# Optimization experiments

Hardware: AMD Instinct MI355X
Metric: run time of the kernel (lower is better)

## Reference

```python
import jax, jax.numpy as jnp
import numpy as np
import math

N_HEADS = 8
TANH_CLIP = 10.0
TEMP = 1.0


def setup_inputs() -> dict:
    key = jax.random.key(0)
    ks = jax.random.split(key, 8)
    B, N, D = 256, 2048, 128
    node_embeddings = jax.random.normal(ks[0], (B, N, D), dtype=jnp.float32)
    W_node = jax.random.normal(ks[1], (D, 3 * D), dtype=jnp.float32) / math.sqrt(D)
    W_fixed = jax.random.normal(ks[2], (D, D), dtype=jnp.float32) / math.sqrt(D)
    W_step = jax.random.normal(ks[3], (2 * D, D), dtype=jnp.float32) / math.sqrt(2 * D)
    W_out = jax.random.normal(ks[4], (D, D), dtype=jnp.float32) / math.sqrt(D)
    first_idx = jax.random.randint(ks[5], (B,), 0, N, dtype=jnp.int32)
    last_idx = jax.random.randint(ks[6], (B,), 0, N, dtype=jnp.int32)
    mask = jax.random.bernoulli(ks[7], 0.5, (B, N))
    mask = mask.at[:, 0].set(False)  # guarantee at least one feasible node per row
    return {"node_embeddings": node_embeddings, "W_node": W_node, "W_fixed": W_fixed,
            "W_step": W_step, "W_out": W_out, "first_idx": first_idx,
            "last_idx": last_idx, "mask": mask}


def reference(node_embeddings, W_node, W_fixed, W_step, W_out, first_idx, last_idx, mask):
    B, N, D = node_embeddings.shape
    H = N_HEADS
    hd = D // H  # key_dim = val_dim = embed_dim / n_heads
    neg_inf = -jnp.inf

    # --- _precompute ---
    graph_embed = node_embeddings.mean(axis=1)                # [B, D]
    fixed_context = graph_embed @ W_fixed                     # [B, D]
    proj = node_embeddings @ W_node                           # [B, N, 3D]
    gK, gV, logit_K = jnp.split(proj, 3, axis=-1)             # each [B, N, D]
    gK = gK.reshape(B, N, H, hd).transpose(2, 0, 1, 3)        # [H, B, N, hd]
    gV = gV.reshape(B, N, H, hd).transpose(2, 0, 1, 3)        # [H, B, N, hd]

    # --- step context: cat(first node emb, last node emb) ---
    first_emb = jnp.take_along_axis(node_embeddings, first_idx[:, None, None].astype(jnp.int32), axis=1)[:, 0]  # [B, D]
    last_emb = jnp.take_along_axis(node_embeddings, last_idx[:, None, None].astype(jnp.int32), axis=1)[:, 0]
    step_ctx = jnp.concatenate([first_emb, last_emb], axis=-1)  # [B, 2D]
    query = fixed_context + step_ctx @ W_step                 # [B, D]

    # --- glimpse multi-head attention (n_query = 1, masked inner) ---
    Q = query.reshape(B, H, hd).transpose(1, 0, 2)            # [H, B, hd]
    compat = jnp.einsum('hbd,hbnd->hbn', Q, gK) / math.sqrt(hd)  # [H, B, N]
    compat = jnp.where(mask[None, :, :], neg_inf, compat)     # mask_inner=True
    attn = jax.nn.softmax(compat, axis=-1)
    heads = jnp.einsum('hbn,hbnd->hbd', attn, gV)             # [H, B, hd]
    glimpse = heads.transpose(1, 0, 2).reshape(B, D) @ W_out  # project_out, [B, D]

    # --- logits with tanh clipping and masking ---
    logits = jnp.einsum('bd,bnd->bn', glimpse, logit_K) / math.sqrt(D)  # [B, N]
    logits = jnp.tanh(logits) * TANH_CLIP
    logits = jnp.where(mask, neg_inf, logits)                 # mask_logits=True
    log_p = jax.nn.log_softmax(logits / TEMP, axis=-1)        # [B, N]
    return log_p
```

## Files before the change

kernel.cpp:

```cpp
#include <hip/hip_runtime.h>
#include <math.h>

#define B_ 256
#define N_ 2048
#define D_ 128
#define GRID_F 1024

#define NEG_HUGE (-1.0e30f)

#define WSE_BYTES ((size_t)B_ * N_ * D_ * 2)
#define WSQ_OFF 262144
#define WSA_OFF 524288
#define WSB_OFF_M 2654208
#define WSC_OFF_M 2658304
#define FLAGS_OFF 2691072
#define WS_NEED_BYTES (WSE_BYTES + (size_t)(FLAGS_OFF + 1280) * 4)

#define WSA_STRIDE 1040
#define FB_WSB_OFF (B_ * 8 * WSA_STRIDE)
#define FB_WSC_OFF (FB_WSB_OFF + B_ * 8 * 2)

typedef __attribute__((ext_vector_type(8))) short bf16x8;
typedef __attribute__((ext_vector_type(4))) float f32x4;
typedef __attribute__((ext_vector_type(4))) unsigned short u16x4;
typedef __attribute__((ext_vector_type(2))) int i32x2;

__device__ __forceinline__ float wave_max64(float v) {
#pragma unroll
  for (int off = 32; off > 0; off >>= 1) v = fmaxf(v, __shfl_xor(v, off, 64));
  return v;
}
__device__ __forceinline__ float wave_sum64(float v) {
#pragma unroll
  for (int off = 32; off > 0; off >>= 1) v += __shfl_xor(v, off, 64);
  return v;
}
__device__ __forceinline__ unsigned short bf16rne(float f) {
  unsigned u = __float_as_uint(f);
  u += 0x7FFFu + ((u >> 16) & 1u);
  return (unsigned short)(u >> 16);
}
__device__ __forceinline__ float bflo(unsigned u) { return __uint_as_float(u << 16); }
__device__ __forceinline__ float bfhi(unsigned u) { return __uint_as_float(u & 0xFFFF0000u); }

__device__ __forceinline__ void do_A(const float* __restrict__ emb,
                                     unsigned short* __restrict__ wsE,
                                     float* __restrict__ wsM, int b, int s, int t,
                                     unsigned char* smem) {
  const int f4 = t & 31, gg = t >> 5;
  const size_t rowbase = (size_t)b * N_;
  float4 acc = make_float4(0.f, 0.f, 0.f, 0.f);
  int n = s * 256 + gg;
#pragma unroll 8
  for (int i = 0; i < 32; ++i, n += 8) {
    const float4 v = *(const float4*)(emb + (rowbase + n) * D_ + f4 * 4);
    acc.x += v.x; acc.y += v.y; acc.z += v.z; acc.w += v.w;
    ushort4 o;
    o.x = bf16rne(v.x); o.y = bf16rne(v.y); o.z = bf16rne(v.z); o.w = bf16rne(v.w);
    *(ushort4*)(wsE + (rowbase + n) * D_ + f4 * 4) = o;
  }
  float4* red = (float4*)smem;
  __syncthreads();
  red[t] = acc;
  __syncthreads();
  if (gg == 0) {
    float4 r = red[f4];
#pragma unroll
    for (int j = 1; j < 8; ++j) {
      const float4 a = red[j * 32 + f4];
      r.x += a.x; r.y += a.y; r.z += a.z; r.w += a.w;
    }
    *(float4*)(wsM + (size_t)(b * 8 + s) * 128 + f4 * 4) = r;
  }
}

__device__ __forceinline__ void do_B(const float* __restrict__ emb,
                                     const float* __restrict__ Wfix,
                                     const float* __restrict__ Wstep,
                                     const float* __restrict__ Wnode,
                                     const int* __restrict__ fidx,
                                     const int* __restrict__ lidx,
                                     const float* __restrict__ wsM,
                                     float* __restrict__ wsQ, int b, int t,
                                     unsigned char* smem) {
  float* ge = (float*)smem;
  float* fe = ge + 128;
  float* le = ge + 256;
  float* pq = ge + 384;
  float* q = ge + 640;
  if (t < 128) {
    float ssum = 0.f;
#pragma unroll
    for (int i = 0; i < 8; ++i) ssum += wsM[(size_t)(b * 8 + i) * 128 + t];
    ge[t] = ssum * (1.0f / 2048.0f);
    fe[t] = emb[((size_t)b * N_ + fidx[b]) * D_ + t];
    le[t] = emb[((size_t)b * N_ + lidx[b]) * D_ + t];
  }
  __syncthreads();
  {
    const int j = t & 127, h2 = t >> 7;
    float acc = 0.f;
#pragma unroll 4
    for (int k = 64 * h2; k < 64 * h2 + 64; ++k) {
      acc = fmaf(ge[k], Wfix[k * 128 + j], acc);
      acc = fmaf(fe[k], Wstep[k * 128 + j], acc);
      acc = fmaf(le[k], Wstep[(128 + k) * 128 + j], acc);
    }
    pq[h2 * 128 + j] = acc;
  }
  __syncthreads();
  if (t < 128) q[t] = pq[t] + pq[128 + t];
  __syncthreads();
  if (t < 128) {
    const float* wrow = Wnode + (size_t)t * 384;
#pragma unroll
    for (int h = 0; h < 8; ++h) {
      float a = 0.f;
#pragma unroll
      for (int k = 0; k < 16; ++k) a = fmaf(q[h * 16 + k], wrow[h * 16 + k], a);
      wsQ[(size_t)b * 1024 + h * 128 + t] = a * 0.25f;
    }
  }
}

__device__ __forceinline__ void do_C(const unsigned short* __restrict__ wsE,
                                     const unsigned char* __restrict__ mask,
                                     const float* __restrict__ wsQ,
                                     float* __restrict__ wsA, int b, int s, int t,
                                     unsigned char* smem) {
  unsigned short* eR = (unsigned short*)smem;
  unsigned short* pT = (unsigned short*)(smem + 18432);
  float* red0 = (float*)(smem + 20736);
  float* red1 = (float*)(smem + 20992);
  float* resc = (float*)(smem + 21248);
  unsigned char* mask_s = smem + 21312;
  const int lane = t & 63, w = t >> 6;
  const int lg = lane >> 4, lc = lane & 15;

  bf16x8 bq[4];
#pragma unroll
  for (int ks = 0; ks < 4; ++ks)
#pragma unroll
    for (int j = 0; j < 8; ++j) bq[ks][j] = 0;
  if (lc < 8) {
    const float* qrow = wsQ + (size_t)b * 1024 + lc * 128;
#pragma unroll
    for (int ks = 0; ks < 4; ++ks)
#pragma unroll
      for (int j = 0; j < 8; ++j)
        bq[ks][j] = (short)bf16rne(qrow[32 * ks + 8 * lg + j]);
  }

  float m_run = -INFINITY, l_run = 0.f;
  f32x4 wacc0 = {0.f, 0.f, 0.f, 0.f}, wacc1 = {0.f, 0.f, 0.f, 0.f};
  const unsigned short* embB = wsE + ((size_t)b * N_ + s * 256) * D_;
  const unsigned char* mrow = mask + (size_t)b * N_ + s * 256;

  for (int tile = 0; tile < 4; ++tile) {
    __syncthreads();
#pragma unroll
    for (int i = 0; i < 4; ++i) {
      const int gid = t + 256 * i;
      const int n = gid >> 4, d0 = (gid & 15) * 8;
      const int widx = ((n >> 2) * 8 + (d0 >> 4)) * 72 + ((n & 3) << 4) + (d0 & 15);
      const uint4 u = *(const uint4*)(embB + ((size_t)tile * 64 + n) * D_ + d0);
      *(uint4*)&eR[widx] = u;
    }
    if (t < 64) mask_s[t] = mrow[tile * 64 + t];
    __syncthreads();

    f32x4 sAcc = {0.f, 0.f, 0.f, 0.f};
#pragma unroll
    for (int ks = 0; ks < 4; ++ks) {
      const int aidx = ((4 * w + (lc >> 2)) * 8 + 2 * ks + (lg >> 1)) * 72 +
                       ((lc & 3) << 4) + ((lg & 1) << 3);
      const bf16x8 af = *(const bf16x8*)&eR[aidx];
      sAcc = __builtin_amdgcn_mfma_f32_16x16x32_bf16(af, bq[ks], sAcc, 0, 0, 0);
    }

    float sv[4];
    bool mk[4];
    float tmax = -INFINITY;
#pragma unroll
    for (int r = 0; r < 4; ++r) {
      mk[r] = mask_s[16 * w + 4 * lg + r] != 0;
      sv[r] = mk[r] ? -INFINITY : sAcc[r];
      tmax = fmaxf(tmax, sv[r]);
    }
    tmax = fmaxf(tmax, __shfl_xor(tmax, 16, 64));
    tmax = fmaxf(tmax, __shfl_xor(tmax, 32, 64));
    if (lane < 16) red0[w * 16 + lc] = tmax;
    __syncthreads();

    const float m_tile = fmaxf(fmaxf(red0[lc], red0[16 + lc]),
                               fmaxf(red0[32 + lc], red0[48 + lc]));
    const float m_new = fmaxf(m_run, m_tile);
    const float rsc = (m_new == -INFINITY) ? 1.f : __expf(m_run - m_new);
    float psum = 0.f;
    unsigned short pu[4];
#pragma unroll
    for (int r = 0; r < 4; ++r) {
      const float p = mk[r] ? 0.f : __expf(sv[r] - m_new);
      psum += p;
      pu[r] = bf16rne(p);
    }
    m_run = m_new;
    psum += __shfl_xor(psum, 16, 64);
    psum += __shfl_xor(psum, 32, 64);
    if (lane < 16) red1[w * 16 + lc] = psum;
    *(u16x4*)&pT[lc * 72 + 16 * w + 4 * lg] = (u16x4){pu[0], pu[1], pu[2], pu[3]};
    if (t < 16) resc[t] = rsc;
    __syncthreads();

    l_run = l_run * rsc + (red1[lc] + red1[16 + lc] + red1[32 + lc] + red1[48 + lc]);
    {
      const float r0f = resc[4 * lg + 0], r1f = resc[4 * lg + 1];
      const float r2f = resc[4 * lg + 2], r3f = resc[4 * lg + 3];
      wacc0[0] *= r0f; wacc0[1] *= r1f; wacc0[2] *= r2f; wacc0[3] *= r3f;
      wacc1[0] *= r0f; wacc1[1] *= r1f; wacc1[2] *= r2f; wacc1[3] *= r3f;
    }

    i32x2 tb0a, tb0b, tb1a, tb1b, tb2a, tb2b, tb3a, tb3b;
    {
      const unsigned base00 = (unsigned)(unsigned long long)
          &eR[((0 + 2 * lg) * 8 + w) * 72 + lc];
      const unsigned base01 = (unsigned)(unsigned long long)
          &eR[((0 + 2 * lg) * 8 + (w + 4)) * 72 + lc];
      const unsigned base10 = (unsigned)(unsigned long long)
          &eR[((8 + 2 * lg) * 8 + w) * 72 + lc];
      const unsigned base11 = (unsigned)(unsigned long long)
          &eR[((8 + 2 * lg) * 8 + (w + 4)) * 72 + lc];
      asm volatile("ds_read_b64_tr_b16 %0, %2 offset:0\n\t"
                   "ds_read_b64_tr_b16 %1, %2 offset:1152"
                   : "=v"(tb0a), "=v"(tb0b) : "v"(base00));
      asm volatile("ds_read_b64_tr_b16 %0, %2 offset:0\n\t"
                   "ds_read_b64_tr_b16 %1, %2 offset:1152"
                   : "=v"(tb1a), "=v"(tb1b) : "v"(base01));
      asm volatile("ds_read_b64_tr_b16 %0, %2 offset:0\n\t"
                   "ds_read_b64_tr_b16 %1, %2 offset:1152"
                   : "=v"(tb2a), "=v"(tb2b) : "v"(base10));
      asm volatile("ds_read_b64_tr_b16 %0, %2 offset:0\n\t"
                   "ds_read_b64_tr_b16 %1, %2 offset:1152"
                   : "=v"(tb3a), "=v"(tb3b) : "v"(base11));
      asm volatile("s_waitcnt lgkmcnt(0)" ::: "memory");
      __builtin_amdgcn_sched_barrier(0);
    }
    {
      const bf16x8 pa0 = *(const bf16x8*)&pT[lc * 72 + 8 * lg];
      const bf16x8 pa1 = *(const bf16x8*)&pT[lc * 72 + 32 + 8 * lg];
      union { i32x2 d[2]; bf16x8 v; } u;
      u.d[0] = tb0a; u.d[1] = tb0b;
      wacc0 = __builtin_amdgcn_mfma_f32_16x16x32_bf16(pa0, u.v, wacc0, 0, 0, 0);
      u.d[0] = tb1a; u.d[1] = tb1b;
      wacc1 = __builtin_amdgcn_mfma_f32_16x16x32_bf16(pa0, u.v, wacc1, 0, 0, 0);
      u.d[0] = tb2a; u.d[1] = tb2b;
      wacc0 = __builtin_amdgcn_mfma_f32_16x16x32_bf16(pa1, u.v, wacc0, 0, 0, 0);
      u.d[0] = tb3a; u.d[1] = tb3b;
      wacc1 = __builtin_amdgcn_mfma_f32_16x16x32_bf16(pa1, u.v, wacc1, 0, 0, 0);
    }
    __syncthreads();
  }

  float* dst = wsA + (size_t)(b * 8 + s) * WSA_STRIDE;
  if (lg < 2) {
#pragma unroll
    for (int r = 0; r < 4; ++r) {
      const int h = 4 * lg + r;
      dst[16 + h * 128 + 16 * w + lc] = wacc0[r];
      dst[16 + h * 128 + 16 * (w + 4) + lc] = wacc1[r];
    }
  }
  if (t < 8) { dst[t] = m_run; dst[8 + t] = l_run; }
}

__device__ __forceinline__ void do_D(const float* __restrict__ Wnode,
                                     const float* __restrict__ Wout,
                                     const float* __restrict__ wsA,
                                     float* __restrict__ wsC, int b, int t,
                                     unsigned char* smem) {
  float* Ls = (float*)smem;
  float* scale = Ls + 8;
  float* wl = scale + 64;
  float* heads = wl + 1024;
  float* glim = heads + 128;
  float* p2 = glim + 128;
  const int j = t & 127, hh = t >> 7;
  const float* base = wsA + (size_t)b * 8 * WSA_STRIDE;

  if (t < 8) {
    float M = -INFINITY;
#pragma unroll
    for (int s = 0; s < 8; ++s) M = fmaxf(M, base[s * WSA_STRIDE + t]);
    float L = 0.f;
#pragma unroll
    for (int s = 0; s < 8; ++s) {
      const float m = base[s * WSA_STRIDE + t];
      const float sc = (m == -INFINITY) ? 0.f : __expf(m - M);
      scale[s * 8 + t] = sc;
      L = fmaf(base[s * WSA_STRIDE + 8 + t], sc, L);
    }
    Ls[t] = L;
  }
  __syncthreads();
#pragma unroll
  for (int k = 0; k < 4; ++k) {
    const int idx = t + 256 * k;
    const int h = idx >> 7, d = idx & 127;
    float acc = 0.f;
#pragma unroll
    for (int s = 0; s < 8; ++s)
      acc = fmaf(scale[s * 8 + h], base[s * WSA_STRIDE + 16 + h * 128 + d], acc);
    wl[idx] = acc;
  }
  __syncthreads();
  {
    const int h = j >> 4, kk = j & 15;
    const float* wp = Wnode + 128 + h * 16 + kk;
    float acc = 0.f;
#pragma unroll 8
    for (int d = 64 * hh; d < 64 * hh + 64; ++d)
      acc = fmaf(wl[h * 128 + d], wp[(size_t)d * 384], acc);
    p2[hh * 128 + j] = acc;
  }
  __syncthreads();
  if (t < 128) heads[t] = (p2[t] + p2[128 + t]) / Ls[t >> 4];
  __syncthreads();
  {
    float acc = 0.f;
#pragma unroll 8
    for (int k = 64 * hh; k < 64 * hh + 64; ++k)
      acc = fmaf(heads[k], Wout[(size_t)k * 128 + j], acc);
    p2[hh * 128 + j] = acc;
  }
  __syncthreads();
  if (t < 128) glim[t] = p2[t] + p2[128 + t];
  __syncthreads();
  {
    const float* wr = Wnode + (size_t)j * 384 + 256;
    float acc = 0.f;
#pragma unroll 8
    for (int k = 64 * hh; k < 64 * hh + 64; ++k) acc = fmaf(wr[k], glim[k], acc);
    p2[hh * 128 + j] = acc;
  }
  __syncthreads();
  if (t < 128)
    wsC[(size_t)b * 128 + t] = (p2[t] + p2[128 + t]) * 0.08838834764831845f;
}

__device__ __forceinline__ void do_E(const unsigned short* __restrict__ wsE,
                                     const unsigned char* __restrict__ mask,
                                     const float* __restrict__ wsC,
                                     float* __restrict__ buf,
                                     float* __restrict__ wsB, int b, int s, int t,
                                     unsigned char* smem) {
  float* lgs = (float*)smem;
  const int lane = t & 63, w4 = t >> 6;
  const float4* c4 = (const float4*)(wsC + (size_t)b * 128);
  const float4 cfa = c4[(t & 15) * 2];
  const float4 cfb = c4[(t & 15) * 2 + 1];
  const unsigned short* embB = wsE + ((size_t)b * N_ + s * 256) * D_;
  const unsigned char* mrow = mask + (size_t)b * N_ + s * 256;
  float mr = NEG_HUGE, sr = 0.f;
  for (int tile = 0; tile < 4; ++tile) {
    const int n0 = tile * 64;
#pragma unroll
    for (int i = 0; i < 4; ++i) {
      const int gid = t + 256 * i;
      const int r = gid >> 4, c8 = (gid & 15) * 8;
      const uint4 u = *(const uint4*)(embB + (size_t)(n0 + r) * D_ + c8);
      float p = bflo(u.x) * cfa.x + bfhi(u.x) * cfa.y;
      p = fmaf(bflo(u.y), cfa.z, p); p = fmaf(bfhi(u.y), cfa.w, p);
      p = fmaf(bflo(u.z), cfb.x, p); p = fmaf(bfhi(u.z), cfb.y, p);
      p = fmaf(bflo(u.w), cfb.z, p); p = fmaf(bfhi(u.w), cfb.w, p);
      p += __shfl_xor(p, 8, 64);
      p += __shfl_xor(p, 4, 64);
      p += __shfl_xor(p, 2, 64);
      p += __shfl_xor(p, 1, 64);
      if ((t & 15) == 0) lgs[r] = p;
    }
    __syncthreads();
    const bool mk = mrow[n0 + lane] != 0;
    const float x = lgs[lane];
    const float ex = __expf(2.f * x);
    const float val = mk ? NEG_HUGE : (10.f - __fdividef(20.f, ex + 1.f));
    const float tm = wave_max64(val);
    const float mn = fmaxf(mr, tm);
    sr = sr * __expf(mr - mn) + wave_sum64(mk ? 0.f : __expf(val - mn));
    mr = mn;
    if (w4 == 0) buf[(size_t)b * N_ + s * 256 + n0 + lane] = val;
    __syncthreads();
  }
  if (t == 0) {
    wsB[(size_t)(b * 8 + s) * 2] = mr;
    wsB[(size_t)(b * 8 + s) * 2 + 1] = sr;
  }
}

__device__ __forceinline__ void do_F(const float* __restrict__ wsB,
                                     float* __restrict__ buf, int b, int t) {
  float M = NEG_HUGE;
#pragma unroll
  for (int q = 0; q < 8; ++q) M = fmaxf(M, wsB[(size_t)(b * 8 + q) * 2]);
  float S = 0.f;
#pragma unroll
  for (int q = 0; q < 8; ++q) {
    const float m = wsB[(size_t)(b * 8 + q) * 2];
    S += wsB[(size_t)(b * 8 + q) * 2 + 1] * __expf(m - M);
  }
  const float LS = M + logf(S);
#pragma unroll
  for (int i = 0; i < 8; ++i) {
    const size_t idx = (size_t)b * N_ + i * 256 + t;
    const float v = buf[idx];
    buf[idx] = (v <= -1.0e29f) ? NEG_HUGE : (v - LS);
  }
}

__global__ void __launch_bounds__(256, 4) k_flow(
    const float* __restrict__ emb, const float* __restrict__ Wnode,
    const float* __restrict__ Wfix, const float* __restrict__ Wstep,
    const float* __restrict__ Wout, const int* __restrict__ fidx,
    const int* __restrict__ lidx, const unsigned char* __restrict__ mask,
    float* __restrict__ buf, unsigned short* __restrict__ wsE,
    float* __restrict__ wsF, unsigned* __restrict__ flg) {
  const int g = blockIdx.x, t = threadIdx.x;
  float* wsM = wsF;
  float* wsQ = wsF + WSQ_OFF;
  float* wsA = wsF + WSA_OFF;
  float* wsB = wsF + WSB_OFF_M;
  float* wsC = wsF + WSC_OFF_M;
  unsigned* aprog = flg;
  unsigned* qrdy = flg + 256;
  unsigned* cprog = flg + 512;
  unsigned* crdy = flg + 768;
  unsigned* eprog = flg + 1024;

  __shared__ __align__(16) unsigned char smem[21504];
  __shared__ unsigned sh_old;

#pragma unroll 1
  for (int pass = 0; pass < 2; ++pass) {
    const int seg = g + GRID_F * pass;
    const int b = seg >> 3, s = seg & 7;

    do_A(emb, wsE, wsM, b, s, t, smem);
    __syncthreads();
    if (t == 0) { __threadfence(); sh_old = atomicAdd(&aprog[b], 1u); }
    __syncthreads();
    if (sh_old == 7u) {
      do_B(emb, Wfix, Wstep, Wnode, fidx, lidx, wsM, wsQ, b, t, smem);
      __syncthreads();
      if (t == 0) { __threadfence(); atomicExch(&qrdy[b], 1u); }
    }

    if (t == 0) {
      while (atomicAdd(&qrdy[b], 0u) == 0u) __builtin_amdgcn_s_sleep(8);
      __threadfence();
    }
    __syncthreads();
    do_C(wsE, mask, wsQ, wsA, b, s, t, smem);
    __syncthreads();
    if (t == 0) { __threadfence(); sh_old = atomicAdd(&cprog[b], 1u); }
    __syncthreads();
    if (sh_old == 7u) {
      do_D(Wnode, Wout, wsA, wsC, b, t, smem);
      __syncthreads();
      if (t == 0) { __threadfence(); atomicExch(&crdy[b], 1u); }
    }

    if (t == 0) {
      while (atomicAdd(&crdy[b], 0u) == 0u) __builtin_amdgcn_s_sleep(8);
      __threadfence();
    }
    __syncthreads();
    do_E(wsE, mask, wsC, buf, wsB, b, s, t, smem);
    __syncthreads();
    if (t == 0) { __threadfence(); sh_old = atomicAdd(&eprog[b], 1u); }
    __syncthreads();
    if (sh_old == 7u) do_F(wsB, buf, b, t);
    __syncthreads();
  }
}

__global__ void __launch_bounds__(256) k_prep(const float* __restrict__ emb,
                                              float* __restrict__ buf) {
  const int b = blockIdx.x, s = blockIdx.y, t = threadIdx.x;
  const int f4 = t & 31, g = t >> 5;
  const size_t rowbase = (size_t)b * N_;
  float4 acc = make_float4(0.f, 0.f, 0.f, 0.f);
  int n = s * 256 + g;
#pragma unroll 8
  for (int i = 0; i < 32; ++i, n += 8) {
    const float4 v = *(const float4*)(emb + (rowbase + n) * D_ + f4 * 4);
    acc.x += v.x; acc.y += v.y; acc.z += v.z; acc.w += v.w;
  }
  __shared__ float4 red[256];
  red[t] = acc;
  __syncthreads();
  if (g == 0) {
    float4 r = red[f4];
#pragma unroll
    for (int j = 1; j < 8; ++j) {
      const float4 a = red[j * 32 + f4];
      r.x += a.x; r.y += a.y; r.z += a.z; r.w += a.w;
    }
    *(float4*)(buf + (size_t)b * N_ + s * 128 + f4 * 4) = r;
  }
}

__global__ void __launch_bounds__(384) k_query(const float* __restrict__ emb,
                                               const float* __restrict__ Wfix,
                                               const float* __restrict__ Wstep,
                                               const float* __restrict__ Wnode,
                                               const int* __restrict__ fidx,
                                               const int* __restrict__ lidx,
                                               float* __restrict__ buf) {
  const int b = blockIdx.x, t = threadIdx.x;
  __shared__ float x[384];
  __shared__ float part[3][128];
  __shared__ float q[128];
  if (t < 128) {
    float ssum = 0.f;
#pragma unroll
    for (int i = 0; i < 8; ++i) ssum += buf[(size_t)b * N_ + i * 128 + t];
    x[t] = ssum * (1.0f / 2048.0f);
  } else if (t < 256) {
    x[t] = emb[((size_t)b * N_ + fidx[b]) * D_ + (t - 128)];
  } else {
    x[t] = emb[((size_t)b * N_ + lidx[b]) * D_ + (t - 256)];
  }
  __syncthreads();
  {
    const int seg = t >> 7, j = t & 127;
    const float* xs = &x[seg * 128];
    const float* Wp = (seg == 0) ? (Wfix + j) : (Wstep + (seg == 1 ? 0 : 128 * 128) + j);
    float acc = 0.f;
#pragma unroll 8
    for (int k = 0; k < 128; ++k) acc = fmaf(xs[k], Wp[(size_t)k * 128], acc);
    part[seg][j] = acc;
  }
  __syncthreads();
  if (t < 128) q[t] = part[0][t] + part[1][t] + part[2][t];
  __syncthreads();
  if (t < 128) {
    const float* wrow = Wnode + (size_t)t * 384;
#pragma unroll
    for (int h = 0; h < 8; ++h) {
      float a = 0.f;
#pragma unroll
      for (int k = 0; k < 16; ++k) a = fmaf(q[h * 16 + k], wrow[h * 16 + k], a);
      buf[(size_t)b * N_ + 1024 + h * 128 + t] = a * 0.25f;
    }
  }
}

__global__ void __launch_bounds__(256) k_attn_m(const float* __restrict__ emb,
                                                const unsigned char* __restrict__ mask,
                                                const float* __restrict__ buf,
                                                float* __restrict__ wsA) {
  const int b = blockIdx.x, s = blockIdx.y;
  const int t = threadIdx.x;
  const int lane = t & 63, w = t >> 6;
  const int lg = lane >> 4, lc = lane & 15;
  __shared__ __align__(16) unsigned char smem[21504];
  unsigned short* eR = (unsigned short*)smem;
  bf16x8 bq[4];
#pragma unroll
  for (int ks = 0; ks < 4; ++ks)
#pragma unroll
    for (int j = 0; j < 8; ++j) bq[ks][j] = 0;
  if (lc < 8) {
    const float* qrow = buf + (size_t)b * N_ + 1024 + lc * 128;
#pragma unroll
    for (int ks = 0; ks < 4; ++ks)
#pragma unroll
      for (int j = 0; j < 8; ++j)
        bq[ks][j] = (short)bf16rne(qrow[32 * ks + 8 * lg + j]);
  }
  unsigned short* pT = (unsigned short*)(smem + 18432);
  float* red0 = (float*)(smem + 20736);
  float* red1 = (float*)(smem + 20992);
  float* resc = (float*)(smem + 21248);
  unsigned char* mask_s = smem + 21312;
  float m_run = -INFINITY, l_run = 0.f;
  f32x4 wacc0 = {0.f, 0.f, 0.f, 0.f}, wacc1 = {0.f, 0.f, 0.f, 0.f};
  const float* embb = emb + ((size_t)b * N_ + s * 256) * D_;
  const unsigned char* mrow = mask + (size_t)b * N_ + s * 256;
  for (int tile = 0; tile < 4; ++tile) {
    {
      const float* src = embb + (size_t)tile * 64 * D_;
#pragma unroll
      for (int i = 0; i < 4; ++i) {
        const int gid = t + 256 * i;
        const int n = gid >> 4, d0 = (gid & 15) * 8;
        const float4 v0 = *(const float4*)(src + (size_t)n * D_ + d0);
        const float4 v1 = *(const float4*)(src + (size_t)n * D_ + d0 + 4);
        bf16x8 ev;
        ev[0] = (short)bf16rne(v0.x); ev[1] = (short)bf16rne(v0.y);
        ev[2] = (short)bf16rne(v0.z); ev[3] = (short)bf16rne(v0.w);
        ev[4] = (short)bf16rne(v1.x); ev[5] = (short)bf16rne(v1.y);
        ev[6] = (short)bf16rne(v1.z); ev[7] = (short)bf16rne(v1.w);
        const int widx = ((n >> 2) * 8 + (d0 >> 4)) * 72 + ((n & 3) << 4) + (d0 & 15);
        *(bf16x8*)&eR[widx] = ev;
      }
      if (t < 64) mask_s[t] = mrow[tile * 64 + t];
    }
    __syncthreads();
    f32x4 sAcc = {0.f, 0.f, 0.f, 0.f};
#pragma unroll
    for (int ks = 0; ks < 4; ++ks) {
      const int aidx = ((4 * w + (lc >> 2)) * 8 + 2 * ks + (lg >> 1)) * 72 +
                       ((lc & 3) << 4) + ((lg & 1) << 3);
      const bf16x8 af = *(const bf16x8*)&eR[aidx];
      sAcc = __builtin_amdgcn_mfma_f32_16x16x32_bf16(af, bq[ks], sAcc, 0, 0, 0);
    }
    float sv[4];
    bool mk[4];
    float tmax = -INFINITY;
#pragma unroll
    for (int r = 0; r < 4; ++r) {
      mk[r] = mask_s[16 * w + 4 * lg + r] != 0;
      sv[r] = mk[r] ? -INFINITY : sAcc[r];
      tmax = fmaxf(tmax, sv[r]);
    }
    tmax = fmaxf(tmax, __shfl_xor(tmax, 16, 64));
    tmax = fmaxf(tmax, __shfl_xor(tmax, 32, 64));
    if (lane < 16) red0[w * 16 + lc] = tmax;
    __syncthreads();
    const float m_tile = fmaxf(fmaxf(red0[lc], red0[16 + lc]),
                               fmaxf(red0[32 + lc], red0[48 + lc]));
    const float m_new = fmaxf(m_run, m_tile);
    const float rsc = (m_new == -INFINITY) ? 1.f : __expf(m_run - m_new);
    float psum = 0.f;
    unsigned short pu[4];
#pragma unroll
    for (int r = 0; r < 4; ++r) {
      const float p = mk[r] ? 0.f : __expf(sv[r] - m_new);
      psum += p;
      pu[r] = bf16rne(p);
    }
    m_run = m_new;
    psum += __shfl_xor(psum, 16, 64);
    psum += __shfl_xor(psum, 32, 64);
    if (lane < 16) red1[w * 16 + lc] = psum;
    *(u16x4*)&pT[lc * 72 + 16 * w + 4 * lg] = (u16x4){pu[0], pu[1], pu[2], pu[3]};
    if (t < 16) resc[t] = rsc;
    __syncthreads();
    l_run = l_run * rsc + (red1[lc] + red1[16 + lc] + red1[32 + lc] + red1[48 + lc]);
    {
      const float r0f = resc[4 * lg + 0], r1f = resc[4 * lg + 1];
      const float r2f = resc[4 * lg + 2], r3f = resc[4 * lg + 3];
      wacc0[0] *= r0f; wacc0[1] *= r1f; wacc0[2] *= r2f; wacc0[3] *= r3f;
      wacc1[0] *= r0f; wacc1[1] *= r1f; wacc1[2] *= r2f; wacc1[3] *= r3f;
    }
    i32x2 tb0a, tb0b, tb1a, tb1b, tb2a, tb2b, tb3a, tb3b;
    {
      const unsigned base00 = (unsigned)(unsigned long long)
          &eR[((0 + 2 * lg) * 8 + w) * 72 + lc];
      const unsigned base01 = (unsigned)(unsigned long long)
          &eR[((0 + 2 * lg) * 8 + (w + 4)) * 72 + lc];
      const unsigned base10 = (unsigned)(unsigned long long)
          &eR[((8 + 2 * lg) * 8 + w) * 72 + lc];
      const unsigned base11 = (unsigned)(unsigned long long)
          &eR[((8 + 2 * lg) * 8 + (w + 4)) * 72 + lc];
      asm volatile("ds_read_b64_tr_b16 %0, %2 offset:0\n\t"
                   "ds_read_b64_tr_b16 %1, %2 offset:1152"
                   : "=v"(tb0a), "=v"(tb0b) : "v"(base00));
      asm volatile("ds_read_b64_tr_b16 %0, %2 offset:0\n\t"
                   "ds_read_b64_tr_b16 %1, %2 offset:1152"
                   : "=v"(tb1a), "=v"(tb1b) : "v"(base01));
      asm volatile("ds_read_b64_tr_b16 %0, %2 offset:0\n\t"
                   "ds_read_b64_tr_b16 %1, %2 offset:1152"
                   : "=v"(tb2a), "=v"(tb2b) : "v"(base10));
      asm volatile("ds_read_b64_tr_b16 %0, %2 offset:0\n\t"
                   "ds_read_b64_tr_b16 %1, %2 offset:1152"
                   : "=v"(tb3a), "=v"(tb3b) : "v"(base11));
      asm volatile("s_waitcnt lgkmcnt(0)" ::: "memory");
      __builtin_amdgcn_sched_barrier(0);
    }
    {
      const bf16x8 pa0 = *(const bf16x8*)&pT[lc * 72 + 8 * lg];
      const bf16x8 pa1 = *(const bf16x8*)&pT[lc * 72 + 32 + 8 * lg];
      union { i32x2 d[2]; bf16x8 v; } u;
      u.d[0] = tb0a; u.d[1] = tb0b;
      wacc0 = __builtin_amdgcn_mfma_f32_16x16x32_bf16(pa0, u.v, wacc0, 0, 0, 0);
      u.d[0] = tb1a; u.d[1] = tb1b;
      wacc1 = __builtin_amdgcn_mfma_f32_16x16x32_bf16(pa0, u.v, wacc1, 0, 0, 0);
      u.d[0] = tb2a; u.d[1] = tb2b;
      wacc0 = __builtin_amdgcn_mfma_f32_16x16x32_bf16(pa1, u.v, wacc0, 0, 0, 0);
      u.d[0] = tb3a; u.d[1] = tb3b;
      wacc1 = __builtin_amdgcn_mfma_f32_16x16x32_bf16(pa1, u.v, wacc1, 0, 0, 0);
    }
    __syncthreads();
  }
  float* dst = wsA + (size_t)(b * 8 + s) * WSA_STRIDE;
  if (lg < 2) {
#pragma unroll
    for (int r = 0; r < 4; ++r) {
      const int h = 4 * lg + r;
      dst[16 + h * 128 + 16 * w + lc] = wacc0[r];
      dst[16 + h * 128 + 16 * (w + 4) + lc] = wacc1[r];
    }
  }
  if (t < 8) { dst[t] = m_run; dst[8 + t] = l_run; }
}

__global__ void __launch_bounds__(256) k_attn_comb(const float* __restrict__ Wnode,
                                                   const float* __restrict__ Wout,
                                                   const float* __restrict__ wsA,
                                                   float* __restrict__ wsC) {
  __shared__ __align__(16) unsigned char smem[10240];
  do_D(Wnode, Wout, wsA, wsC, blockIdx.x, threadIdx.x, smem);
}

__global__ void __launch_bounds__(256) k_logits_part(const float* __restrict__ emb,
                                                     const unsigned char* __restrict__ mask,
                                                     const float* __restrict__ wsC,
                                                     float* __restrict__ buf,
                                                     float* __restrict__ wsB) {
  const int b = blockIdx.x, s = blockIdx.y;
  const int t = threadIdx.x, lane = t & 63, w = t >> 6;
  __shared__ float lg[64];
  const float4 cf = ((const float4*)(wsC + (size_t)b * 128))[t & 31];
  const float* embb = emb + ((size_t)b * N_ + s * 256) * D_;
  const unsigned char* mrow = mask + (size_t)b * N_ + s * 256;
  float mr = NEG_HUGE, sr = 0.f;
  for (int tile = 0; tile < 4; ++tile) {
    const int n0 = tile * 64;
#pragma unroll
    for (int i = 0; i < 8; ++i) {
      const int gid = t + 256 * i;
      const int r = gid >> 5, c = (gid & 31) * 4;
      const float4 e = *(const float4*)(embb + (size_t)(n0 + r) * D_ + c);
      float p = fmaf(e.x, cf.x, fmaf(e.y, cf.y, fmaf(e.z, cf.z, e.w * cf.w)));
      p += __shfl_xor(p, 16, 64);
      p += __shfl_xor(p, 8, 64);
      p += __shfl_xor(p, 4, 64);
      p += __shfl_xor(p, 2, 64);
      p += __shfl_xor(p, 1, 64);
      if ((t & 31) == 0) lg[r] = p;
    }
    __syncthreads();
    const bool mk = mrow[n0 + lane] != 0;
    const float x = lg[lane];
    const float ex = __expf(2.f * x);
    const float val = mk ? NEG_HUGE : (10.f - __fdividef(20.f, ex + 1.f));
    const float tm = wave_max64(val);
    const float mn = fmaxf(mr, tm);
    sr = sr * __expf(mr - mn) + wave_sum64(mk ? 0.f : __expf(val - mn));
    mr = mn;
    if (w == 0) buf[(size_t)b * N_ + s * 256 + n0 + lane] = val;
    __syncthreads();
  }
  if (t == 0) {
    wsB[(size_t)(b * 8 + s) * 2] = mr;
    wsB[(size_t)(b * 8 + s) * 2 + 1] = sr;
  }
}

__global__ void __launch_bounds__(256) k_norm(const float* __restrict__ wsB,
                                              float* __restrict__ buf) {
  const int b = blockIdx.x, s = blockIdx.y, t = threadIdx.x;
  float M = NEG_HUGE;
#pragma unroll
  for (int q = 0; q < 8; ++q) M = fmaxf(M, wsB[(size_t)(b * 8 + q) * 2]);
  float S = 0.f;
#pragma unroll
  for (int q = 0; q < 8; ++q) {
    const float m = wsB[(size_t)(b * 8 + q) * 2];
    S += wsB[(size_t)(b * 8 + q) * 2 + 1] * __expf(m - M);
  }
  const float LS = M + logf(S);
  const size_t idx = (size_t)b * N_ + s * 256 + t;
  const float v = buf[idx];
  buf[idx] = (v <= -1.0e29f) ? NEG_HUGE : (v - LS);
}

extern "C" void kernel_launch(void* const* d_in, const int* in_sizes, int n_in,
                              void* d_out, int out_size, void* d_ws, size_t ws_size,
                              hipStream_t stream) {
  (void)in_sizes; (void)n_in; (void)out_size;
  const float* emb = (const float*)d_in[0];
  const float* Wnode = (const float*)d_in[1];
  const float* Wfix = (const float*)d_in[2];
  const float* Wstep = (const float*)d_in[3];
  const float* Wout = (const float*)d_in[4];
  const int* fidx = (const int*)d_in[5];
  const int* lidx = (const int*)d_in[6];
  const unsigned char* mask = (const unsigned char*)d_in[7];
  float* buf = (float*)d_out;

  int occ = 0;
  (void)hipOccupancyMaxActiveBlocksPerMultiprocessor(&occ, k_flow, 256, 0);

  if (occ >= 4 && ws_size >= WS_NEED_BYTES) {
    unsigned short* wsE = (unsigned short*)d_ws;
    float* wsF = (float*)((char*)d_ws + WSE_BYTES);
    unsigned* flg = (unsigned*)(wsF + FLAGS_OFF);
    hipMemsetAsync(flg, 0, 1280 * 4, stream);
    k_flow<<<GRID_F, 256, 0, stream>>>(emb, Wnode, Wfix, Wstep, Wout, fidx,
                                       lidx, mask, buf, wsE, wsF, flg);
  } else {
    float* ws = (float*)d_ws;
    k_prep<<<dim3(B_, 8), 256, 0, stream>>>(emb, buf);
    k_query<<<B_, 384, 0, stream>>>(emb, Wfix, Wstep, Wnode, fidx, lidx, buf);
    k_attn_m<<<dim3(B_, 8), 256, 0, stream>>>(emb, mask, buf, ws);
    k_attn_comb<<<B_, 256, 0, stream>>>(Wnode, Wout, ws, ws + FB_WSC_OFF);
    k_logits_part<<<dim3(B_, 8), 256, 0, stream>>>(emb, mask, ws + FB_WSC_OFF, buf,
                                                   ws + FB_WSB_OFF);
    k_norm<<<dim3(B_, 8), 256, 0, stream>>>(ws + FB_WSB_OFF, buf);
  }
}
```

Baseline: 160.3 us.

## Keep bf16 segment in LDS across fused persistent passes instead of global workspace

Replaces the persistent flow kernel, which staged a bf16 copy of all embeddings in global workspace, with a fused kernel. Each block converts a 256-node segment into a 72KB LDS buffer and reuses it for the mean, the attention and the logits phases within the same pass. This removes the global bf16 write and its two re-reads, leaving one read of the fp32 input. The cost is lower occupancy (2 blocks per CU, grid of 512), so each block runs 4 passes. Each pass also spin-waits on per-batch flags, which risks stalls while that segment's LDS buffer stays resident.

```diff
diff --git a/kernel.cpp b/kernel.cpp
--- a/kernel.cpp
+++ b/kernel.cpp
@@ -4,17 +4,16 @@
 #define B_ 256
 #define N_ 2048
 #define D_ 128
-#define GRID_F 1024
+#define GRID_F 512
 
 #define NEG_HUGE (-1.0e30f)
 
-#define WSE_BYTES ((size_t)B_ * N_ * D_ * 2)
 #define WSQ_OFF 262144
 #define WSA_OFF 524288
 #define WSB_OFF_M 2654208
 #define WSC_OFF_M 2658304
 #define FLAGS_OFF 2691072
-#define WS_NEED_BYTES (WSE_BYTES + (size_t)(FLAGS_OFF + 1280) * 4)
+#define WS_NEED_BYTES ((size_t)(FLAGS_OFF + 1280) * 4)
 
 #define WSA_STRIDE 1040
 #define FB_WSB_OFF (B_ * 8 * WSA_STRIDE)
@@ -43,73 +42,479 @@
 __device__ __forceinline__ float bflo(unsigned u) { return __uint_as_float(u << 16); }
 __device__ __forceinline__ float bfhi(unsigned u) { return __uint_as_float(u & 0xFFFF0000u); }
 
-__device__ __forceinline__ void do_A(const float* __restrict__ emb,
-                                     unsigned short* __restrict__ wsE,
-                                     float* __restrict__ wsM, int b, int s, int t,
+__device__ __forceinline__ void do_D(const float* __restrict__ Wnode,
+                                     const float* __restrict__ Wout,
+                                     const float* __restrict__ wsA,
+                                     float* __restrict__ wsC, int b, int t,
                                      unsigned char* smem) {
-  const int f4 = t & 31, gg = t >> 5;
+  float* Ls = (float*)smem;
+  float* scale = Ls + 8;
+  float* wl = scale + 64;
+  float* heads = wl + 1024;
+  float* glim = heads + 128;
+  float* p2 = glim + 128;
+  const int j = t & 127, hh = t >> 7;
+  const float* base = wsA + (size_t)b * 8 * WSA_STRIDE;
+
+  if (t < 8) {
+    float M = -INFINITY;
+#pragma unroll
+    for (int s = 0; s < 8; ++s) M = fmaxf(M, base[s * WSA_STRIDE + t]);
+    float L = 0.f;
+#pragma unroll
+    for (int s = 0; s < 8; ++s) {
+      const float m = base[s * WSA_STRIDE + t];
+      const float sc = (m == -INFINITY) ? 0.f : __expf(m - M);
+      scale[s * 8 + t] = sc;
+      L = fmaf(base[s * WSA_STRIDE + 8 + t], sc, L);
+    }
+    Ls[t] = L;
+  }
+  __syncthreads();
+#pragma unroll
+  for (int k = 0; k < 4; ++k) {
+    const int idx = t + 256 * k;
+    const int h = idx >> 7, d = idx & 127;
+    float acc = 0.f;
+#pragma unroll
+    for (int s = 0; s < 8; ++s)
+      acc = fmaf(scale[s * 8 + h], base[s * WSA_STRIDE + 16 + h * 128 + d], acc);
+    wl[idx] = acc;
+  }
+  __syncthreads();
+  {
+    const int h = j >> 4, kk = j & 15;
+    const float* wp = Wnode + 128 + h * 16 + kk;
+    float acc = 0.f;
+#pragma unroll 8
+    for (int d = 64 * hh; d < 64 * hh + 64; ++d)
+      acc = fmaf(wl[h * 128 + d], wp[(size_t)d * 384], acc);
+    p2[hh * 128 + j] = acc;
+  }
+  __syncthreads();
+  if (t < 128) heads[t] = (p2[t] + p2[128 + t]) / Ls[t >> 4];
+  __syncthreads();
+  {
+    float acc = 0.f;
+#pragma unroll 8
+    for (int k = 64 * hh; k < 64 * hh + 64; ++k)
+      acc = fmaf(heads[k], Wout[(size_t)k * 128 + j], acc);
+    p2[hh * 128 + j] = acc;
+  }
+  __syncthreads();
+  if (t < 128) glim[t] = p2[t] + p2[128 + t];
+  __syncthreads();
+  {
+    const float* wr = Wnode + (size_t)j * 384 + 256;
+    float acc = 0.f;
+#pragma unroll 8
+    for (int k = 64 * hh; k < 64 * hh + 64; ++k) acc = fmaf(wr[k], glim[k], acc);
+    p2[hh * 128 + j] = acc;
+  }
+  __syncthreads();
+  if (t < 128)
+    wsC[(size_t)b * 128 + t] = (p2[t] + p2[128 + t]) * 0.08838834764831845f;
+  __syncthreads();
+}
+
+__global__ void __launch_bounds__(256, 2) k_fused(
+    const float* __restrict__ emb, const float* __restrict__ Wnode,
+    const float* __restrict__ Wfix, const float* __restrict__ Wstep,
+    const float* __restrict__ Wout, const int* __restrict__ fidx,
+    const int* __restrict__ lidx, const unsigned char* __restrict__ mask,
+    float* __restrict__ buf, float* __restrict__ wsF,
+    unsigned* __restrict__ flg) {
+  const int g = blockIdx.x, t = threadIdx.x;
+  float* wsM = wsF;
+  float* wsQ = wsF + WSQ_OFF;
+  float* wsA = wsF + WSA_OFF;
+  float* wsB = wsF + WSB_OFF_M;
+  float* wsC = wsF + WSC_OFF_M;
+  unsigned* aprog = flg;
+  unsigned* qrdy = flg + 256;
+  unsigned* cprog = flg + 512;
+  unsigned* crdy = flg + 768;
+  unsigned* eprog = flg + 1024;
+
+  __shared__ __align__(16) unsigned short eSeg[36864];
+  __shared__ __align__(16) unsigned char scratch[6464];
+  __shared__ unsigned sh_old;
+
+  const int lane = t & 63, w = t >> 6;
+  const int lg = lane >> 4, lc = lane & 15;
+
+#pragma unroll 1
+  for (int pass = 0; pass < 4; ++pass) {
+    const int seg = g + GRID_F * pass;
+    const int b = seg >> 3, s = seg & 7;
+    const float* src = emb + ((size_t)b * N_ + s * 256) * D_;
+    const unsigned char* mrow = mask + (size_t)b * N_ + s * 256;
+
+    {
+      const int d0 = (t & 15) * 8;
+      float p[8];
+#pragma unroll
+      for (int j = 0; j < 8; ++j) p[j] = 0.f;
+#pragma unroll
+      for (int i = 0; i < 16; ++i) {
+        const int n = (t >> 4) + 16 * i;
+        const float4 v0 = *(const float4*)(src + (size_t)n * D_ + d0);
+        const float4 v1 = *(const float4*)(src + (size_t)n * D_ + d0 + 4);
+        p[0] += v0.x; p[1] += v0.y; p[2] += v0.z; p[3] += v0.w;
+        p[4] += v1.x; p[5] += v1.y; p[6] += v1.z; p[7] += v1.w;
+        bf16x8 ev;
+        ev[0] = (short)bf16rne(v0.x); ev[1] = (short)bf16rne(v0.y);
+        ev[2] = (short)bf16rne(v0.z); ev[3] = (short)bf16rne(v0.w);
+        ev[4] = (short)bf16rne(v1.x); ev[5] = (short)bf16rne(v1.y);
+        ev[6] = (short)bf16rne(v1.z); ev[7] = (short)bf16rne(v1.w);
+        const int widx = ((n >> 2) * 8 + (d0 >> 4)) * 72 + ((n & 3) << 4) + (d0 & 15);
+        *(bf16x8*)&eSeg[widx] = ev;
+      }
+#pragma unroll
+      for (int j = 0; j < 8; ++j) {
+        p[j] += __shfl_xor(p[j], 16, 64);
+        p[j] += __shfl_xor(p[j], 32, 64);
+      }
+      float* red = (float*)scratch;
+      if (lane < 16) {
+        float* dstp = red + w * 128 + lane * 8;
+#pragma unroll
+        for (int j = 0; j < 8; ++j) dstp[j] = p[j];
+      }
+      __syncthreads();
+      if (t < 128)
+        wsM[(size_t)(b * 8 + s) * 128 + t] =
+            red[t] + red[128 + t] + red[256 + t] + red[384 + t];
+      __syncthreads();
+    }
+    if (t == 0) { __threadfence(); sh_old = atomicAdd(&aprog[b], 1u); }
+    __syncthreads();
+
+    if (sh_old == 7u) {
+      __threadfence();
+      float* ge = (float*)scratch;
+      float* fe = ge + 128;
+      float* le = ge + 256;
+      float* pq = ge + 384;
+      float* q = ge + 640;
+      if (t < 128) {
+        float ssum = 0.f;
+#pragma unroll
+        for (int i = 0; i < 8; ++i) ssum += wsM[(size_t)(b * 8 + i) * 128 + t];
+        ge[t] = ssum * (1.0f / 2048.0f);
+        fe[t] = emb[((size_t)b * N_ + fidx[b]) * D_ + t];
+        le[t] = emb[((size_t)b * N_ + lidx[b]) * D_ + t];
+      }
+      __syncthreads();
+      {
+        const int j = t & 127, h2 = t >> 7;
+        float acc = 0.f;
+#pragma unroll 4
+        for (int k = 64 * h2; k < 64 * h2 + 64; ++k) {
+          acc = fmaf(ge[k], Wfix[k * 128 + j], acc);
+          acc = fmaf(fe[k], Wstep[k * 128 + j], acc);
+          acc = fmaf(le[k], Wstep[(128 + k) * 128 + j], acc);
+        }
+        pq[h2 * 128 + j] = acc;
+      }
+      __syncthreads();
+      if (t < 128) q[t] = pq[t] + pq[128 + t];
+      __syncthreads();
+      if (t < 128) {
+        const float* wrow = Wnode + (size_t)t * 384;
+#pragma unroll
+        for (int h = 0; h < 8; ++h) {
+          float a = 0.f;
+#pragma unroll
+          for (int k = 0; k < 16; ++k) a = fmaf(q[h * 16 + k], wrow[h * 16 + k], a);
+          wsQ[(size_t)b * 1024 + h * 128 + t] = a * 0.25f;
+        }
+      }
+      __syncthreads();
+      if (t == 0) { __threadfence(); atomicExch(&qrdy[b], 1u); }
+    }
+
+    if (t == 0) {
+      while (atomicAdd(&qrdy[b], 0u) == 0u) __builtin_amdgcn_s_sleep(8);
+      __threadfence();
+    }
+    __syncthreads();
+    {
+      unsigned short* pT = (unsigned short*)scratch;
+      float* red0 = (float*)(scratch + 2304);
+      float* red1 = (float*)(scratch + 2560);
+      float* resc = (float*)(scratch + 2816);
+
+      bf16x8 bq[4];
+#pragma unroll
+      for (int ks = 0; ks < 4; ++ks)
+#pragma unroll
+        for (int j = 0; j < 8; ++j) bq[ks][j] = 0;
+      if (lc < 8) {
+        const float* qrow = wsQ + (size_t)b * 1024 + lc * 128;
+#pragma unroll
+        for (int ks = 0; ks < 4; ++ks)
+#pragma unroll
+          for (int j = 0; j < 8; ++j)
+            bq[ks][j] = (short)bf16rne(qrow[32 * ks + 8 * lg + j]);
+      }
+
+      float m_run = -INFINITY, l_run = 0.f;
+      f32x4 wacc0 = {0.f, 0.f, 0.f, 0.f}, wacc1 = {0.f, 0.f, 0.f, 0.f};
+
+      for (int tile = 0; tile < 4; ++tile) {
+        const unsigned short* eR = eSeg + tile * 9216;
+        __syncthreads();
+
+        f32x4 sAcc = {0.f, 0.f, 0.f, 0.f};
+#pragma unroll
+        for (int ks = 0; ks < 4; ++ks) {
+          const int aidx = ((4 * w + (lc >> 2)) * 8 + 2 * ks + (lg >> 1)) * 72 +
+                           ((lc & 3) << 4) + ((lg & 1) << 3);
+          const bf16x8 af = *(const bf16x8*)&eR[aidx];
+          sAcc = __builtin_amdgcn_mfma_f32_16x16x32_bf16(af, bq[ks], sAcc, 0, 0, 0);
+        }
+
+        float sv[4];
+        bool mk[4];
+        float tmax = -INFINITY;
+#pragma unroll
+        for (int r = 0; r < 4; ++r) {
+          mk[r] = mrow[tile * 64 + 16 * w + 4 * lg + r] != 0;
+          sv[r] = mk[r] ? -INFINITY : sAcc[r];
+          tmax = fmaxf(tmax, sv[r]);
+        }
+        tmax = fmaxf(tmax, __shfl_xor(tmax, 16, 64));
+        tmax = fmaxf(tmax, __shfl_xor(tmax, 32, 64));
+        if (lane < 16) red0[w * 16 + lc] = tmax;
+        __syncthreads();
+
+        const float m_tile = fmaxf(fmaxf(red0[lc], red0[16 + lc]),
+                                   fmaxf(red0[32 + lc], red0[48 + lc]));
+        const float m_new = fmaxf(m_run, m_tile);
+        const float rsc = (m_new == -INFINITY) ? 1.f : __expf(m_run - m_new);
+        float psum = 0.f;
+        unsigned short pu[4];
+#pragma unroll
+        for (int r = 0; r < 4; ++r) {
+          const float p = mk[r] ? 0.f : __expf(sv[r] - m_new);
+          psum += p;
+          pu[r] = bf16rne(p);
+        }
+        m_run = m_new;
+        psum += __shfl_xor(psum, 16, 64);
+        psum += __shfl_xor(psum, 32, 64);
+        if (lane < 16) red1[w * 16 + lc] = psum;
+        *(u16x4*)&pT[lc * 72 + 16 * w + 4 * lg] = (u16x4){pu[0], pu[1], pu[2], pu[3]};
+        if (t < 16) resc[t] = rsc;
+        __syncthreads();
+
+        l_run = l_run * rsc +
+                (red1[lc] + red1[16 + lc] + red1[32 + lc] + red1[48 + lc]);
+        {
+          const float r0f = resc[4 * lg + 0], r1f = resc[4 * lg + 1];
+          const float r2f = resc[4 * lg + 2], r3f = resc[4 * lg + 3];
+          wacc0[0] *= r0f; wacc0[1] *= r1f; wacc0[2] *= r2f; wacc0[3] *= r3f;
+          wacc1[0] *= r0f; wacc1[1] *= r1f; wacc1[2] *= r2f; wacc1[3] *= r3f;
+        }
+
+        i32x2 tb0a, tb0b, tb1a, tb1b, tb2a, tb2b, tb3a, tb3b;
+        {
+          const unsigned base00 = (unsigned)(unsigned long long)
+              &eR[((0 + 2 * lg) * 8 + w) * 72 + lc];
+          const unsigned base01 = (unsigned)(unsigned long long)
+              &eR[((0 + 2 * lg) * 8 + (w + 4)) * 72 + lc];
+          const unsigned base10 = (unsigned)(unsigned long long)
+              &eR[((8 + 2 * lg) * 8 + w) * 72 + lc];
+          const unsigned base11 = (unsigned)(unsigned long long)
+              &eR[((8 + 2 * lg) * 8 + (w + 4)) * 72 + lc];
+          asm volatile("ds_read_b64_tr_b16 %0, %2 offset:0\n\t"
+                       "ds_read_b64_tr_b16 %1, %2 offset:1152"
+                       : "=v"(tb0a), "=v"(tb0b) : "v"(base00));
+          asm volatile("ds_read_b64_tr_b16 %0, %2 offset:0\n\t"
+                       "ds_read_b64_tr_b16 %1, %2 offset:1152"
+                       : "=v"(tb1a), "=v"(tb1b) : "v"(base01));
+          asm volatile("ds_read_b64_tr_b16 %0, %2 offset:0\n\t"
+                       "ds_read_b64_tr_b16 %1, %2 offset:1152"
+                       : "=v"(tb2a), "=v"(tb2b) : "v"(base10));
+          asm volatile("ds_read_b64_tr_b16 %0, %2 offset:0\n\t"
+                       "ds_read_b64_tr_b16 %1, %2 offset:1152"
+                       : "=v"(tb3a), "=v"(tb3b) : "v"(base11));
+          asm volatile("s_waitcnt lgkmcnt(0)" ::: "memory");
+          __builtin_amdgcn_sched_barrier(0);
+        }
+        {
+          const bf16x8 pa0 = *(const bf16x8*)&pT[lc * 72 + 8 * lg];
+          const bf16x8 pa1 = *(const bf16x8*)&pT[lc * 72 + 32 + 8 * lg];
+          union { i32x2 d[2]; bf16x8 v; } u;
+          u.d[0] = tb0a; u.d[1] = tb0b;
+          wacc0 = __builtin_amdgcn_mfma_f32_16x16x32_bf16(pa0, u.v, wacc0, 0, 0, 0);
+          u.d[0] = tb1a; u.d[1] = tb1b;
+          wacc1 = __builtin_amdgcn_mfma_f32_16x16x32_bf16(pa0, u.v, wacc1, 0, 0, 0);
+          u.d[0] = tb2a; u.d[1] = tb2b;
+          wacc0 = __builtin_amdgcn_mfma_f32_16x16x32_bf16(pa1, u.v, wacc0, 0, 0, 0);
+          u.d[0] = tb3a; u.d[1] = tb3b;
+          wacc1 = __builtin_amdgcn_mfma_f32_16x16x32_bf16(pa1, u.v, wacc1, 0, 0, 0);
+        }
+      }
+      __syncthreads();
+
+      float* dst = wsA + (size_t)(b * 8 + s) * WSA_STRIDE;
+      if (lg < 2) {
+#pragma unroll
+        for (int r = 0; r < 4; ++r) {
+          const int h = 4 * lg + r;
+          dst[16 + h * 128 + 16 * w + lc] = wacc0[r];
+          dst[16 + h * 128 + 16 * (w + 4) + lc] = wacc1[r];
+        }
+      }
+      if (t < 8) { dst[t] = m_run; dst[8 + t] = l_run; }
+    }
+    __syncthreads();
+    if (t == 0) { __threadfence(); sh_old = atomicAdd(&cprog[b], 1u); }
+    __syncthreads();
+
+    if (sh_old == 7u) {
+      __threadfence();
+      do_D(Wnode, Wout, wsA, wsC, b, t, scratch);
+      if (t == 0) { __threadfence(); atomicExch(&crdy[b], 1u); }
+    }
+
+    if (t == 0) {
+      while (atomicAdd(&crdy[b], 0u) == 0u) __builtin_amdgcn_s_sleep(8);
+      __threadfence();
+    }
+    __syncthreads();
+    {
+      float* lgs = (float*)scratch;
+      const float4* c4 = (const float4*)(wsC + (size_t)b * 128);
+      const float4 cfa = c4[(t & 15) * 2];
+      const float4 cfb = c4[(t & 15) * 2 + 1];
+      float mr = NEG_HUGE, sr = 0.f;
+      for (int tile = 0; tile < 4; ++tile) {
+        const int n0 = tile * 64;
+#pragma unroll
+        for (int i = 0; i < 4; ++i) {
+          const int gid = t + 256 * i;
+          const int r = gid >> 4, c8 = (gid & 15) * 8;
+          const int nn = n0 + r;
+          const int idx =
+              ((nn >> 2) * 8 + (c8 >> 4)) * 72 + ((nn & 3) << 4) + (c8 & 15);
+          const bf16x8 ev = *(const bf16x8*)&eSeg[idx];
+          const uint4 u = *(const uint4*)&ev;
+          float p = bflo(u.x) * cfa.x + bfhi(u.x) * cfa.y;
+          p = fmaf(bflo(u.y), cfa.z, p); p = fmaf(bfhi(u.y), cfa.w, p);
+          p = fmaf(bflo(u.z), cfb.x, p); p = fmaf(bfhi(u.z), cfb.y, p);
+          p = fmaf(bflo(u.w), cfb.z, p); p = fmaf(bfhi(u.w), cfb.w, p);
+          p += __shfl_xor(p, 8, 64);
+          p += __shfl_xor(p, 4, 64);
+          p += __shfl_xor(p, 2, 64);
+          p += __shfl_xor(p, 1, 64);
+          if ((t & 15) == 0) lgs[r] = p;
+        }
+        __syncthreads();
+        const bool mk = mrow[n0 + lane] != 0;
+        const float x = lgs[lane];
+        const float ex = __expf(2.f * x);
+        const float val = mk ? NEG_HUGE : (10.f - __fdividef(20.f, ex + 1.f));
+        const float tm = wave_max64(val);
+        const float mn = fmaxf(mr, tm);
+        sr = sr * __expf(mr - mn) + wave_sum64(mk ? 0.f : __expf(val - mn));
+        mr = mn;
+        if (w == 0) buf[(size_t)b * N_ + s * 256 + n0 + lane] = val;
+        __syncthreads();
+      }
+      if (t == 0) {
+        wsB[(size_t)(b * 8 + s) * 2] = mr;
+        wsB[(size_t)(b * 8 + s) * 2 + 1] = sr;
+      }
+    }
+    __syncthreads();
+    if (t == 0) { __threadfence(); sh_old = atomicAdd(&eprog[b], 1u); }
+    __syncthreads();
+
+    if (sh_old == 7u) {
+      __threadfence();
+      float M = NEG_HUGE;
+#pragma unroll
+      for (int q = 0; q < 8; ++q) M = fmaxf(M, wsB[(size_t)(b * 8 + q) * 2]);
+      float S = 0.f;
+#pragma unroll
+      for (int q = 0; q < 8; ++q) {
+        const float m = wsB[(size_t)(b * 8 + q) * 2];
+        S += wsB[(size_t)(b * 8 + q) * 2 + 1] * __expf(m - M);
+      }
+      const float LS = M + logf(S);
+#pragma unroll
+      for (int i = 0; i < 8; ++i) {
+        const size_t idx = (size_t)b * N_ + i * 256 + t;
+        const float v = buf[idx];
+        buf[idx] = (v <= -1.0e29f) ? NEG_HUGE : (v - LS);
+      }
+    }
+    __syncthreads();
+  }
+}
+
+__global__ void __launch_bounds__(256) k_prep(const float* __restrict__ emb,
+                                              float* __restrict__ buf) {
+  const int b = blockIdx.x, s = blockIdx.y, t = threadIdx.x;
+  const int f4 = t & 31, g = t >> 5;
   const size_t rowbase = (size_t)b * N_;
   float4 acc = make_float4(0.f, 0.f, 0.f, 0.f);
-  int n = s * 256 + gg;
+  int n = s * 256 + g;
 #pragma unroll 8
   for (int i = 0; i < 32; ++i, n += 8) {
     const float4 v = *(const float4*)(emb + (rowbase + n) * D_ + f4 * 4);
     acc.x += v.x; acc.y += v.y; acc.z += v.z; acc.w += v.w;
-    ushort4 o;
-    o.x = bf16rne(v.x); o.y = bf16rne(v.y); o.z = bf16rne(v.z); o.w = bf16rne(v.w);
-    *(ushort4*)(wsE + (rowbase + n) * D_ + f4 * 4) = o;
-  }
-  float4* red = (float4*)smem;
-  __syncthreads();
+  }
+  __shared__ float4 red[256];
   red[t] = acc;
   __syncthreads();
-  if (gg == 0) {
+  if (g == 0) {
     float4 r = red[f4];
 #pragma unroll
     for (int j = 1; j < 8; ++j) {
       const float4 a = red[j * 32 + f4];
       r.x += a.x; r.y += a.y; r.z += a.z; r.w += a.w;
     }
-    *(float4*)(wsM + (size_t)(b * 8 + s) * 128 + f4 * 4) = r;
-  }
-}
-
-__device__ __forceinline__ void do_B(const float* __restrict__ emb,
-                                     const float* __restrict__ Wfix,
-                                     const float* __restrict__ Wstep,
-                                     const float* __restrict__ Wnode,
-                                     const int* __restrict__ fidx,
-                                     const int* __restrict__ lidx,
-                                     const float* __restrict__ wsM,
-                                     float* __restrict__ wsQ, int b, int t,
-                                     unsigned char* smem) {
-  float* ge = (float*)smem;
-  float* fe = ge + 128;
-  float* le = ge + 256;
-  float* pq = ge + 384;
-  float* q = ge + 640;
+    *(float4*)(buf + (size_t)b * N_ + s * 128 + f4 * 4) = r;
+  }
+}
+
+__global__ void __launch_bounds__(384) k_query(const float* __restrict__ emb,
+                                               const float* __restrict__ Wfix,
+                                               const float* __restrict__ Wstep,
+                                               const float* __restrict__ Wnode,
+                                               const int* __restrict__ fidx,
+                                               const int* __restrict__ lidx,
+                                               float* __restrict__ buf) {
+  const int b = blockIdx.x, t = threadIdx.x;
+  __shared__ float x[384];
+  __shared__ float part[3][128];
+  __shared__ float q[128];
   if (t < 128) {
     float ssum = 0.f;
 #pragma unroll
-    for (int i = 0; i < 8; ++i) ssum += wsM[(size_t)(b * 8 + i) * 128 + t];
-    ge[t] = ssum * (1.0f / 2048.0f);
-    fe[t] = emb[((size_t)b * N_ + fidx[b]) * D_ + t];
-    le[t] = emb[((size_t)b * N_ + lidx[b]) * D_ + t];
+    for (int i = 0; i < 8; ++i) ssum += buf[(size_t)b * N_ + i * 128 + t];
+    x[t] = ssum * (1.0f / 2048.0f);
+  } else if (t < 256) {
+    x[t] = emb[((size_t)b * N_ + fidx[b]) * D_ + (t - 128)];
+  } else {
+    x[t] = emb[((size_t)b * N_ + lidx[b]) * D_ + (t - 256)];
   }
   __syncthreads();
   {
-    const int j = t & 127, h2 = t >> 7;
+    const int seg = t >> 7, j = t & 127;
+    const float* xs = &x[seg * 128];
+    const float* Wp = (seg == 0) ? (Wfix + j) : (Wstep + (seg == 1 ? 0 : 128 * 128) + j);
     float acc = 0.f;
-#pragma unroll 4
-    for (int k = 64 * h2; k < 64 * h2 + 64; ++k) {
-      acc = fmaf(ge[k], Wfix[k * 128 + j], acc);
-      acc = fmaf(fe[k], Wstep[k * 128 + j], acc);
-      acc = fmaf(le[k], Wstep[(128 + k) * 128 + j], acc);
-    }
-    pq[h2 * 128 + j] = acc;
-  }
-  __syncthreads();
-  if (t < 128) q[t] = pq[t] + pq[128 + t];
+#pragma unroll 8
+    for (int k = 0; k < 128; ++k) acc = fmaf(xs[k], Wp[(size_t)k * 128], acc);
+    part[seg][j] = acc;
+  }
+  __syncthreads();
+  if (t < 128) q[t] = part[0][t] + part[1][t] + part[2][t];
   __syncthreads();
   if (t < 128) {
     const float* wrow = Wnode + (size_t)t * 384;
@@ -118,57 +523,62 @@
       float a = 0.f;
 #pragma unroll
       for (int k = 0; k < 16; ++k) a = fmaf(q[h * 16 + k], wrow[h * 16 + k], a);
-      wsQ[(size_t)b * 1024 + h * 128 + t] = a * 0.25f;
-    }
-  }
-}
-
-__device__ __forceinline__ void do_C(const unsigned short* __restrict__ wsE,
-                                     const unsigned char* __restrict__ mask,
-                                     const float* __restrict__ wsQ,
-                                     float* __restrict__ wsA, int b, int s, int t,
-                                     unsigned char* smem) {
-  unsigned short* eR = (unsigned short*)smem;
-  unsigned short* pT = (unsigned short*)(smem + 18432);
-  float* red0 = (float*)(smem + 20736);
-  float* red1 = (float*)(smem + 20992);
-  float* resc = (float*)(smem + 21248);
-  unsigned char* mask_s = smem + 21312;
+      buf[(size_t)b * N_ + 1024 + h * 128 + t] = a * 0.25f;
+    }
+  }
+}
+
+__global__ void __launch_bounds__(256) k_attn_m(const float* __restrict__ emb,
+                                                const unsigned char* __restrict__ mask,
+                                                const float* __restrict__ buf,
+                                                float* __restrict__ wsA) {
+  const int b = blockIdx.x, s = blockIdx.y;
+  const int t = threadIdx.x;
   const int lane = t & 63, w = t >> 6;
   const int lg = lane >> 4, lc = lane & 15;
-
+  __shared__ __align__(16) unsigned short eR[9216];
+  __shared__ __align__(16) unsigned short pT[16 * 72];
+  __shared__ float red0[64];
+  __shared__ float red1[64];
+  __shared__ float resc[16];
+  __shared__ unsigned char mask_s[64];
   bf16x8 bq[4];
 #pragma unroll
   for (int ks = 0; ks < 4; ++ks)
 #pragma unroll
     for (int j = 0; j < 8; ++j) bq[ks][j] = 0;
   if (lc < 8) {
-    const float* qrow = wsQ + (size_t)b * 1024 + lc * 128;
+    const float* qrow = buf + (size_t)b * N_ + 1024 + lc * 128;
 #pragma unroll
     for (int ks = 0; ks < 4; ++ks)
 #pragma unroll
       for (int j = 0; j < 8; ++j)
         bq[ks][j] = (short)bf16rne(qrow[32 * ks + 8 * lg + j]);
   }
-
   float m_run = -INFINITY, l_run = 0.f;
   f32x4 wacc0 = {0.f, 0.f, 0.f, 0.f}, wacc1 = {0.f, 0.f, 0.f, 0.f};
-  const unsigned short* embB = wsE + ((size_t)b * N_ + s * 256) * D_;
+  const float* embb = emb + ((size_t)b * N_ + s * 256) * D_;
   const unsigned char* mrow = mask + (size_t)b * N_ + s * 256;
-
   for (int tile = 0; tile < 4; ++tile) {
-    __syncthreads();
-#pragma unroll
-    for (int i = 0; i < 4; ++i) {
-      const int gid = t + 256 * i;
-      const int n = gid >> 4, d0 = (gid & 15) * 8;
-      const int widx = ((n >> 2) * 8 + (d0 >> 4)) * 72 + ((n & 3) << 4) + (d0 & 15);
-      const uint4 u = *(const uint4*)(embB + ((size_t)tile * 64 + n) * D_ + d0);
-      *(uint4*)&eR[widx] = u;
-    }
-    if (t < 64) mask_s[t] = mrow[tile * 64 + t];
-    __syncthreads();
-
+    {
+      const float* src = embb + (size_t)tile * 64 * D_;
+#pragma unroll
+      for (int i = 0; i < 4; ++i) {
+        const int gid = t + 256 * i;
+        const int n = gid >> 4, d0 = (gid & 15) * 8;
+        const float4 v0 = *(const float4*)(src + (size_t)n * D_ + d0);
+        const float4 v1 = *(const float4*)(src + (size_t)n * D_ + d0 + 4);
+        bf16x8 ev;
+        ev[0] = (short)bf16rne(v0.x); ev[1] = (short)bf16rne(v0.y);
+        ev[2] = (short)bf16rne(v0.z); ev[3] = (short)bf16rne(v0.w);
+        ev[4] = (short)bf16rne(v1.x); ev[5] = (short)bf16rne(v1.y);
+        ev[6] = (short)bf16rne(v1.z); ev[7] = (short)bf16rne(v1.w);
+        const int widx = ((n >> 2) * 8 + (d0 >> 4)) * 72 + ((n & 3) << 4) + (d0 & 15);
+        *(bf16x8*)&eR[widx] = ev;
+      }
+      if (t < 64) mask_s[t] = mrow[tile * 64 + t];
+    }
+    __syncthreads();
     f32x4 sAcc = {0.f, 0.f, 0.f, 0.f};
 #pragma unroll
     for (int ks = 0; ks < 4; ++ks) {
@@ -177,7 +587,6 @@
       const bf16x8 af = *(const bf16x8*)&eR[aidx];
       sAcc = __builtin_amdgcn_mfma_f32_16x16x32_bf16(af, bq[ks], sAcc, 0, 0, 0);
     }
-
     float sv[4];
     bool mk[4];
     float tmax = -INFINITY;
@@ -191,7 +600,6 @@
     tmax = fmaxf(tmax, __shfl_xor(tmax, 32, 64));
     if (lane < 16) red0[w * 16 + lc] = tmax;
     __syncthreads();
-
     const float m_tile = fmaxf(fmaxf(red0[lc], red0[16 + lc]),
                                fmaxf(red0[32 + lc], red0[48 + lc]));
     const float m_new = fmaxf(m_run, m_tile);
@@ -211,7 +619,6 @@
     *(u16x4*)&pT[lc * 72 + 16 * w + 4 * lg] = (u16x4){pu[0], pu[1], pu[2], pu[3]};
     if (t < 16) resc[t] = rsc;
     __syncthreads();
-
     l_run = l_run * rsc + (red1[lc] + red1[16 + lc] + red1[32 + lc] + red1[48 + lc]);
     {
       const float r0f = resc[4 * lg + 0], r1f = resc[4 * lg + 1];
@@ -219,7 +626,6 @@
       wacc0[0] *= r0f; wacc0[1] *= r1f; wacc0[2] *= r2f; wacc0[3] *= r3f;
       wacc1[0] *= r0f; wacc1[1] *= r1f; wacc1[2] *= r2f; wacc1[3] *= r3f;
     }
-
     i32x2 tb0a, tb0b, tb1a, tb1b, tb2a, tb2b, tb3a, tb3b;
     {
       const unsigned base00 = (unsigned)(unsigned long long)
@@ -260,7 +666,6 @@
     }
     __syncthreads();
   }
-
   float* dst = wsA + (size_t)(b * 8 + s) * WSA_STRIDE;
   if (lg < 2) {
 #pragma unroll
@@ -273,443 +678,11 @@
   if (t < 8) { dst[t] = m_run; dst[8 + t] = l_run; }
 }
 
-__device__ __forceinline__ void do_D(const float* __restrict__ Wnode,
-                                     const float* __restrict__ Wout,
-                                     const float* __restrict__ wsA,
-                                     float* __restrict__ wsC, int b, int t,
-                                     unsigned char* smem) {
-  float* Ls = (float*)smem;
-  float* scale = Ls + 8;
-  float* wl = scale + 64;
-  float* heads = wl + 1024;
-  float* glim = heads + 128;
-  float* p2 = glim + 128;
-  const int j = t & 127, hh = t >> 7;
-  const float* base = wsA + (size_t)b * 8 * WSA_STRIDE;
-
-  if (t < 8) {
-    float M = -INFINITY;
-#pragma unroll
-    for (int s = 0; s < 8; ++s) M = fmaxf(M, base[s * WSA_STRIDE + t]);
-    float L = 0.f;
-#pragma unroll
-    for (int s = 0; s < 8; ++s) {
-      const float m = base[s * WSA_STRIDE + t];
-      const float sc = (m == -INFINITY) ? 0.f : __expf(m - M);
-      scale[s * 8 + t] = sc;
-      L = fmaf(base[s * WSA_STRIDE + 8 + t], sc, L);
-    }
-    Ls[t] = L;
-  }
-  __syncthreads();
-#pragma unroll
-  for (int k = 0; k < 4; ++k) {
-    const int idx = t + 256 * k;
-    const int h = idx >> 7, d = idx & 127;
-    float acc = 0.f;
-#pragma unroll
-    for (int s = 0; s < 8; ++s)
-      acc = fmaf(scale[s * 8 + h], base[s * WSA_STRIDE + 16 + h * 128 + d], acc);
-    wl[idx] = acc;
-  }
-  __syncthreads();
-  {
-    const int h = j >> 4, kk = j & 15;
-    const float* wp = Wnode + 128 + h * 16 + kk;
-    float acc = 0.f;
-#pragma unroll 8
-    for (int d = 64 * hh; d < 64 * hh + 64; ++d)
-      acc = fmaf(wl[h * 128 + d], wp[(size_t)d * 384], acc);
-    p2[hh * 128 + j] = acc;
-  }
-  __syncthreads();
-  if (t < 128) heads[t] = (p2[t] + p2[128 + t]) / Ls[t >> 4];
-  __syncthreads();
-  {
-    float acc = 0.f;
-#pragma unroll 8
-    for (int k = 64 * hh; k < 64 * hh + 64; ++k)
-      acc = fmaf(heads[k], Wout[(size_t)k * 128 + j], acc);
-    p2[hh * 128 + j] = acc;
-  }
-  __syncthreads();
-  if (t < 128) glim[t] = p2[t] + p2[128 + t];
-  __syncthreads();
-  {
-    const float* wr = Wnode + (size_t)j * 384 + 256;
-    float acc = 0.f;
-#pragma unroll 8
-    for (int k = 64 * hh; k < 64 * hh + 64; ++k) acc = fmaf(wr[k], glim[k], acc);
-    p2[hh * 128 + j] = acc;
-  }
-  __syncthreads();
-  if (t < 128)
-    wsC[(size_t)b * 128 + t] = (p2[t] + p2[128 + t]) * 0.08838834764831845f;
-}
-
-__device__ __forceinline__ void do_E(const unsigned short* __restrict__ wsE,
-                                     const unsigned char* __restrict__ mask,
-                                     const float* __restrict__ wsC,
-                                     float* __restrict__ buf,
-                                     float* __restrict__ wsB, int b, int s, int t,
-                                     unsigned char* smem) {
-  float* lgs = (float*)smem;
-  const int lane = t & 63, w4 = t >> 6;
-  const float4* c4 = (const float4*)(wsC + (size_t)b * 128);
-  const float4 cfa = c4[(t & 15) * 2];
-  const float4 cfb = c4[(t & 15) * 2 + 1];
-  const unsigned short* embB = wsE + ((size_t)b * N_ + s * 256) * D_;
-  const unsigned char* mrow = mask + (size_t)b * N_ + s * 256;
-  float mr = NEG_HUGE, sr = 0.f;
-  for (int tile = 0; tile < 4; ++tile) {
-    const int n0 = tile * 64;
-#pragma unroll
-    for (int i = 0; i < 4; ++i) {
-      const int gid = t + 256 * i;
-      const int r = gid >> 4, c8 = (gid & 15) * 8;
-      const uint4 u = *(const uint4*)(embB + (size_t)(n0 + r) * D_ + c8);
-      float p = bflo(u.x) * cfa.x + bfhi(u.x) * cfa.y;
-      p = fmaf(bflo(u.y), cfa.z, p); p = fmaf(bfhi(u.y), cfa.w, p);
-      p = fmaf(bflo(u.z), cfb.x, p); p = fmaf(bfhi(u.z), cfb.y, p);
-      p = fmaf(bflo(u.w), cfb.z, p); p = fmaf(bfhi(u.w), cfb.w, p);
-      p += __shfl_xor(p, 8, 64);
-      p += __shfl_xor(p, 4, 64);
-      p += __shfl_xor(p, 2, 64);
-      p += __shfl_xor(p, 1, 64);
-      if ((t & 15) == 0) lgs[r] = p;
-    }
-    __syncthreads();
-    const bool mk = mrow[n0 + lane] != 0;
-    const float x = lgs[lane];
-    const float ex = __expf(2.f * x);
-    const float val = mk ? NEG_HUGE : (10.f - __fdividef(20.f, ex + 1.f));
-    const float tm = wave_max64(val);
-    const float mn = fmaxf(mr, tm);
-    sr = sr * __expf(mr - mn) + wave_sum64(mk ? 0.f : __expf(val - mn));
-    mr = mn;
-    if (w4 == 0) buf[(size_t)b * N_ + s * 256 + n0 + lane] = val;
-    __syncthreads();
-  }
-  if (t == 0) {
-    wsB[(size_t)(b * 8 + s) * 2] = mr;
-    wsB[(size_t)(b * 8 + s) * 2 + 1] = sr;
-  }
-}
-
-__device__ __forceinline__ void do_F(const float* __restrict__ wsB,
-                                     float* __restrict__ buf, int b, int t) {
-  float M = NEG_HUGE;
-#pragma unroll
-  for (int q = 0; q < 8; ++q) M = fmaxf(M, wsB[(size_t)(b * 8 + q) * 2]);
-  float S = 0.f;
-#pragma unroll
-  for (int q = 0; q < 8; ++q) {
-    const float m = wsB[(size_t)(b * 8 + q) * 2];
-    S += wsB[(size_t)(b * 8 + q) * 2 + 1] * __expf(m - M);
-  }
-  const float LS = M + logf(S);
-#pragma unroll
-  for (int i = 0; i < 8; ++i) {
-    const size_t idx = (size_t)b * N_ + i * 256 + t;
-    const float v = buf[idx];
-    buf[idx] = (v <= -1.0e29f) ? NEG_HUGE : (v - LS);
-  }
-}
-
-__global__ void __launch_bounds__(256, 4) k_flow(
-    const float* __restrict__ emb, const float* __restrict__ Wnode,
-    const float* __restrict__ Wfix, const float* __restrict__ Wstep,
-    const float* __restrict__ Wout, const int* __restrict__ fidx,
-    const int* __restrict__ lidx, const unsigned char* __restrict__ mask,
-    float* __restrict__ buf, unsigned short* __restrict__ wsE,
-    float* __restrict__ wsF, unsigned* __restrict__ flg) {
-  const int g = blockIdx.x, t = threadIdx.x;
-  float* wsM = wsF;
-  float* wsQ = wsF + WSQ_OFF;
-  float* wsA = wsF + WSA_OFF;
-  float* wsB = wsF + WSB_OFF_M;
-  float* wsC = wsF + WSC_OFF_M;
-  unsigned* aprog = flg;
-  unsigned* qrdy = flg + 256;
-  unsigned* cprog = flg + 512;
-  unsigned* crdy = flg + 768;
-  unsigned* eprog = flg + 1024;
-
-  __shared__ __align__(16) unsigned char smem[21504];
-  __shared__ unsigned sh_old;
-
-#pragma unroll 1
-  for (int pass = 0; pass < 2; ++pass) {
-    const int seg = g + GRID_F * pass;
-    const int b = seg >> 3, s = seg & 7;
-
-    do_A(emb, wsE, wsM, b, s, t, smem);
-    __syncthreads();
-    if (t == 0) { __threadfence(); sh_old = atomicAdd(&aprog[b], 1u); }
-    __syncthreads();
-    if (sh_old == 7u) {
-      do_B(emb, Wfix, Wstep, Wnode, fidx, lidx, wsM, wsQ, b, t, smem);
-      __syncthreads();
-      if (t == 0) { __threadfence(); atomicExch(&qrdy[b], 1u); }
-    }
-
-    if (t == 0) {
-      while (atomicAdd(&qrdy[b], 0u) == 0u) __builtin_amdgcn_s_sleep(8);
-      __threadfence();
-    }
-    __syncthreads();
-    do_C(wsE, mask, wsQ, wsA, b, s, t, smem);
-    __syncthreads();
-    if (t == 0) { __threadfence(); sh_old = atomicAdd(&cprog[b], 1u); }
-    __syncthreads();
-    if (sh_old == 7u) {
-      do_D(Wnode, Wout, wsA, wsC, b, t, smem);
-      __syncthreads();
-      if (t == 0) { __threadfence(); atomicExch(&crdy[b], 1u); }
-    }
-
-    if (t == 0) {
-      while (atomicAdd(&crdy[b], 0u) == 0u) __builtin_amdgcn_s_sleep(8);
-      __threadfence();
-    }
-    __syncthreads();
-    do_E(wsE, mask, wsC, buf, wsB, b, s, t, smem);
-    __syncthreads();
-    if (t == 0) { __threadfence(); sh_old = atomicAdd(&eprog[b], 1u); }
-    __syncthreads();
-    if (sh_old == 7u) do_F(wsB, buf, b, t);
-    __syncthreads();
-  }
-}
-
-__global__ void __launch_bounds__(256) k_prep(const float* __restrict__ emb,
-                                              float* __restrict__ buf) {
-  const int b = blockIdx.x, s = blockIdx.y, t = threadIdx.x;
-  const int f4 = t & 31, g = t >> 5;
-  const size_t rowbase = (size_t)b * N_;
-  float4 acc = make_float4(0.f, 0.f, 0.f, 0.f);
-  int n = s * 256 + g;
-#pragma unroll 8
-  for (int i = 0; i < 32; ++i, n += 8) {
-    const float4 v = *(const float4*)(emb + (rowbase + n) * D_ + f4 * 4);
-    acc.x += v.x; acc.y += v.y; acc.z += v.z; acc.w += v.w;
-  }
-  __shared__ float4 red[256];
-  red[t] = acc;
-  __syncthreads();
-  if (g == 0) {
-    float4 r = red[f4];
-#pragma unroll
-    for (int j = 1; j < 8; ++j) {
-      const float4 a = red[j * 32 + f4];
-      r.x += a.x; r.y += a.y; r.z += a.z; r.w += a.w;
-    }
-    *(float4*)(buf + (size_t)b * N_ + s * 128 + f4 * 4) = r;
-  }
-}
-
-__global__ void __launch_bounds__(384) k_query(const float* __restrict__ emb,
-                                               const float* __restrict__ Wfix,
-                                               const float* __restrict__ Wstep,
-                                               const float* __restrict__ Wnode,
-                                               const int* __restrict__ fidx,
-                                               const int* __restrict__ lidx,
-                                               float* __restrict__ buf) {
-  const int b = blockIdx.x, t = threadIdx.x;
-  __shared__ float x[384];
-  __shared__ float part[3][128];
-  __shared__ float q[128];
-  if (t < 128) {
-    float ssum = 0.f;
-#pragma unroll
-    for (int i = 0; i < 8; ++i) ssum += buf[(size_t)b * N_ + i * 128 + t];
-    x[t] = ssum * (1.0f / 2048.0f);
-  } else if (t < 256) {
-    x[t] = emb[((size_t)b * N_ + fidx[b]) * D_ + (t - 128)];
-  } else {
-    x[t] = emb[((size_t)b * N_ + lidx[b]) * D_ + (t - 256)];
-  }
-  __syncthreads();
-  {
-    const int seg = t >> 7, j = t & 127;
-    const float* xs = &x[seg * 128];
-    const float* Wp = (seg == 0) ? (Wfix + j) : (Wstep + (seg == 1 ? 0 : 128 * 128) + j);
-    float acc = 0.f;
-#pragma unroll 8
-    for (int k = 0; k < 128; ++k) acc = fmaf(xs[k], Wp[(size_t)k * 128], acc);
-    part[seg][j] = acc;
-  }
-  __syncthreads();
-  if (t < 128) q[t] = part[0][t] + part[1][t] + part[2][t];
-  __syncthreads();
-  if (t < 128) {
-    const float* wrow = Wnode + (size_t)t * 384;
-#pragma unroll
-    for (int h = 0; h < 8; ++h) {
-      float a = 0.f;
-#pragma unroll
-      for (int k = 0; k < 16; ++k) a = fmaf(q[h * 16 + k], wrow[h * 16 + k], a);
-      buf[(size_t)b * N_ + 1024 + h * 128 + t] = a * 0.25f;
-    }
-  }
-}
-
-__global__ void __launch_bounds__(256) k_attn_m(const float* __restrict__ emb,
-                                                const unsigned char* __restrict__ mask,
-                                                const float* __restrict__ buf,
-                                                float* __restrict__ wsA) {
-  const int b = blockIdx.x, s = blockIdx.y;
-  const int t = threadIdx.x;
-  const int lane = t & 63, w = t >> 6;
-  const int lg = lane >> 4, lc = lane & 15;
-  __shared__ __align__(16) unsigned char smem[21504];
-  unsigned short* eR = (unsigned short*)smem;
-  bf16x8 bq[4];
-#pragma unroll
-  for (int ks = 0; ks < 4; ++ks)
-#pragma unroll
-    for (int j = 0; j < 8; ++j) bq[ks][j] = 0;
-  if (lc < 8) {
-    const float* qrow = buf + (size_t)b * N_ + 1024 + lc * 128;
-#pragma unroll
-    for (int ks = 0; ks < 4; ++ks)
-#pragma unroll
-      for (int j = 0; j < 8; ++j)
-        bq[ks][j] = (short)bf16rne(qrow[32 * ks + 8 * lg + j]);
-  }
-  unsigned short* pT = (unsigned short*)(smem + 18432);
-  float* red0 = (float*)(smem + 20736);
-  float* red1 = (float*)(smem + 20992);
-  float* resc = (float*)(smem + 21248);
-  unsigned char* mask_s = smem + 21312;
-  float m_run = -INFINITY, l_run = 0.f;
-  f32x4 wacc0 = {0.f, 0.f, 0.f, 0.f}, wacc1 = {0.f, 0.f, 0.f, 0.f};
-  const float* embb = emb + ((size_t)b * N_ + s * 256) * D_;
-  const unsigned char* mrow = mask + (size_t)b * N_ + s * 256;
-  for (int tile = 0; tile < 4; ++tile) {
-    {
-      const float* src = embb + (size_t)tile * 64 * D_;
-#pragma unroll
-      for (int i = 0; i < 4; ++i) {
-        const int gid = t + 256 * i;
-        const int n = gid >> 4, d0 = (gid & 15) * 8;
-        const float4 v0 = *(const float4*)(src + (size_t)n * D_ + d0);
-        const float4 v1 = *(const float4*)(src + (size_t)n * D_ + d0 + 4);
-        bf16x8 ev;
-        ev[0] = (short)bf16rne(v0.x); ev[1] = (short)bf16rne(v0.y);
-        ev[2] = (short)bf16rne(v0.z); ev[3] = (short)bf16rne(v0.w);
-        ev[4] = (short)bf16rne(v1.x); ev[5] = (short)bf16rne(v1.y);
-        ev[6] = (short)bf16rne(v1.z); ev[7] = (short)bf16rne(v1.w);
-        const int widx = ((n >> 2) * 8 + (d0 >> 4)) * 72 + ((n & 3) << 4) + (d0 & 15);
-        *(bf16x8*)&eR[widx] = ev;
-      }
-      if (t < 64) mask_s[t] = mrow[tile * 64 + t];
-    }
-    __syncthreads();
-    f32x4 sAcc = {0.f, 0.f, 0.f, 0.f};
-#pragma unroll
-    for (int ks = 0; ks < 4; ++ks) {
-      const int aidx = ((4 * w + (lc >> 2)) * 8 + 2 * ks + (lg >> 1)) * 72 +
-                       ((lc & 3) << 4) + ((lg & 1) << 3);
-      const bf16x8 af = *(const bf16x8*)&eR[aidx];
-      sAcc = __builtin_amdgcn_mfma_f32_16x16x32_bf16(af, bq[ks], sAcc, 0, 0, 0);
-    }
-    float sv[4];
-    bool mk[4];
-    float tmax = -INFINITY;
-#pragma unroll
-    for (int r = 0; r < 4; ++r) {
-      mk[r] = mask_s[16 * w + 4 * lg + r] != 0;
-      sv[r] = mk[r] ? -INFINITY : sAcc[r];
-      tmax = fmaxf(tmax, sv[r]);
-    }
-    tmax = fmaxf(tmax, __shfl_xor(tmax, 16, 64));
-    tmax = fmaxf(tmax, __shfl_xor(tmax, 32, 64));
-    if (lane < 16) red0[w * 16 + lc] = tmax;
-    __syncthreads();
-    const float m_tile = fmaxf(fmaxf(red0[lc], red0[16 + lc]),
-                               fmaxf(red0[32 + lc], red0[48 + lc]));
-    const float m_new = fmaxf(m_run, m_tile);
-    const float rsc = (m_new == -INFINITY) ? 1.f : __expf(m_run - m_new);
-    float psum = 0.f;
-    unsigned short pu[4];
-#pragma unroll
-    for (int r = 0; r < 4; ++r) {
-      const float p = mk[r] ? 0.f : __expf(sv[r] - m_new);
-      psum += p;
-      pu[r] = bf16rne(p);
-    }
-    m_run = m_new;
-    psum += __shfl_xor(psum, 16, 64);
-    psum += __shfl_xor(psum, 32, 64);
-    if (lane < 16) red1[w * 16 + lc] = psum;
-    *(u16x4*)&pT[lc * 72 + 16 * w + 4 * lg] = (u16x4){pu[0], pu[1], pu[2], pu[3]};
-    if (t < 16) resc[t] = rsc;
-    __syncthreads();
-    l_run = l_run * rsc + (red1[lc] + red1[16 + lc] + red1[32 + lc] + red1[48 + lc]);
-    {
-      const float r0f = resc[4 * lg + 0], r1f = resc[4 * lg + 1];
-      const float r2f = resc[4 * lg + 2], r3f = resc[4 * lg + 3];
-      wacc0[0] *= r0f; wacc0[1] *= r1f; wacc0[2] *= r2f; wacc0[3] *= r3f;
-      wacc1[0] *= r0f; wacc1[1] *= r1f; wacc1[2] *= r2f; wacc1[3] *= r3f;
-    }
-    i32x2 tb0a, tb0b, tb1a, tb1b, tb2a, tb2b, tb3a, tb3b;
-    {
-      const unsigned base00 = (unsigned)(unsigned long long)
-          &eR[((0 + 2 * lg) * 8 + w) * 72 + lc];
-      const unsigned base01 = (unsigned)(unsigned long long)
-          &eR[((0 + 2 * lg) * 8 + (w + 4)) * 72 + lc];
-      const unsigned base10 = (unsigned)(unsigned long long)
-          &eR[((8 + 2 * lg) * 8 + w) * 72 + lc];
-      const unsigned base11 = (unsigned)(unsigned long long)
-          &eR[((8 + 2 * lg) * 8 + (w + 4)) * 72 + lc];
-      asm volatile("ds_read_b64_tr_b16 %0, %2 offset:0\n\t"
-                   "ds_read_b64_tr_b16 %1, %2 offset:1152"
-                   : "=v"(tb0a), "=v"(tb0b) : "v"(base00));
-      asm volatile("ds_read_b64_tr_b16 %0, %2 offset:0\n\t"
-                   "ds_read_b64_tr_b16 %1, %2 offset:1152"
-                   : "=v"(tb1a), "=v"(tb1b) : "v"(base01));
-      asm volatile("ds_read_b64_tr_b16 %0, %2 offset:0\n\t"
-                   "ds_read_b64_tr_b16 %1, %2 offset:1152"
-                   : "=v"(tb2a), "=v"(tb2b) : "v"(base10));
-      asm volatile("ds_read_b64_tr_b16 %0, %2 offset:0\n\t"
-                   "ds_read_b64_tr_b16 %1, %2 offset:1152"
-                   : "=v"(tb3a), "=v"(tb3b) : "v"(base11));
-      asm volatile("s_waitcnt lgkmcnt(0)" ::: "memory");
-      __builtin_amdgcn_sched_barrier(0);
-    }
-    {
-      const bf16x8 pa0 = *(const bf16x8*)&pT[lc * 72 + 8 * lg];
-      const bf16x8 pa1 = *(const bf16x8*)&pT[lc * 72 + 32 + 8 * lg];
-      union { i32x2 d[2]; bf16x8 v; } u;
-      u.d[0] = tb0a; u.d[1] = tb0b;
-      wacc0 = __builtin_amdgcn_mfma_f32_16x16x32_bf16(pa0, u.v, wacc0, 0, 0, 0);
-      u.d[0] = tb1a; u.d[1] = tb1b;
-      wacc1 = __builtin_amdgcn_mfma_f32_16x16x32_bf16(pa0, u.v, wacc1, 0, 0, 0);
-      u.d[0] = tb2a; u.d[1] = tb2b;
-      wacc0 = __builtin_amdgcn_mfma_f32_16x16x32_bf16(pa1, u.v, wacc0, 0, 0, 0);
-      u.d[0] = tb3a; u.d[1] = tb3b;
-      wacc1 = __builtin_amdgcn_mfma_f32_16x16x32_bf16(pa1, u.v, wacc1, 0, 0, 0);
-    }
-    __syncthreads();
-  }
-  float* dst = wsA + (size_t)(b * 8 + s) * WSA_STRIDE;
-  if (lg < 2) {
-#pragma unroll
-    for (int r = 0; r < 4; ++r) {
-      const int h = 4 * lg + r;
-      dst[16 + h * 128 + 16 * w + lc] = wacc0[r];
-      dst[16 + h * 128 + 16 * (w + 4) + lc] = wacc1[r];
-    }
-  }
-  if (t < 8) { dst[t] = m_run; dst[8 + t] = l_run; }
-}
-
 __global__ void __launch_bounds__(256) k_attn_comb(const float* __restrict__ Wnode,
                                                    const float* __restrict__ Wout,
                                                    const float* __restrict__ wsA,
                                                    float* __restrict__ wsC) {
-  __shared__ __align__(16) unsigned char smem[10240];
+  __shared__ __align__(16) unsigned char smem[6464];
   do_D(Wnode, Wout, wsA, wsC, blockIdx.x, threadIdx.x, smem);
 }
 
@@ -791,15 +764,14 @@
   float* buf = (float*)d_out;
 
   int occ = 0;
-  (void)hipOccupancyMaxActiveBlocksPerMultiprocessor(&occ, k_flow, 256, 0);
-
-  if (occ >= 4 && ws_size >= WS_NEED_BYTES) {
-    unsigned short* wsE = (unsigned short*)d_ws;
-    float* wsF = (float*)((char*)d_ws + WSE_BYTES);
+  (void)hipOccupancyMaxActiveBlocksPerMultiprocessor(&occ, k_fused, 256, 0);
+
+  if (occ >= 2 && ws_size >= WS_NEED_BYTES) {
+    float* wsF = (float*)d_ws;
     unsigned* flg = (unsigned*)(wsF + FLAGS_OFF);
     hipMemsetAsync(flg, 0, 1280 * 4, stream);
-    k_flow<<<GRID_F, 256, 0, stream>>>(emb, Wnode, Wfix, Wstep, Wout, fidx,
-                                       lidx, mask, buf, wsE, wsF, flg);
+    k_fused<<<GRID_F, 256, 0, stream>>>(emb, Wnode, Wfix, Wstep, Wout, fidx,
+                                        lidx, mask, buf, wsF, flg);
   } else {
     float* ws = (float*)d_ws;
     k_prep<<<dim3(B_, 8), 256, 0, stream>>>(emb, buf);
```

Result: no change. 160.8 us (+0.3%).
